# Optimization experiments

Measured on AMD Instinct MI355X. Metric: run time of the kernel, lower is better.

The kernel has to match this reference:

```python
import jax, jax.numpy as jnp
import numpy as np

ND, NPR, DD, DP, LAT, AT, B = 2048, 2048, 128, 128, 128, 32, 16384


def setup_inputs():
    key = jax.random.key(0)
    ks = jax.random.split(key, 20)
    s = 0.05
    d = {}
    d["e_p_adj"] = (jax.random.uniform(ks[0], (ND, NPR)) < 0.05).astype(jnp.float32)
    d["e_e_adj"] = (jax.random.uniform(ks[1], (ND, ND)) < 0.05).astype(jnp.float32)
    d["p_p_adj"] = (jax.random.uniform(ks[2], (NPR, NPR)) < 0.05).astype(jnp.float32)
    d["input_disease"] = jax.random.randint(ks[3], (B,), 0, ND)
    d["input_drug"] = jax.random.randint(ks[4], (B,), 0, NPR)
    d["labels"] = jax.random.randint(ks[5], (B,), 0, 2)
    # learned parameters
    d["disease_emb"] = jax.random.normal(ks[6], (ND, DD)) * s
    d["drug_emb"] = jax.random.normal(ks[7], (NPR, DP)) * s
    d["Wdg"] = jax.random.normal(ks[8], (DP, LAT)) * s   # disease_gcn_w
    d["bdg_lin"] = jnp.zeros((LAT,))                      # Linear bias
    d["bdg"] = jnp.zeros((LAT,))                          # extra disease_gcn_b
    d["Wpg"] = jax.random.normal(ks[9], (DD, LAT)) * s   # drug_gcn_w
    d["bpg_lin"] = jnp.zeros((LAT,))
    d["bpg"] = jnp.zeros((LAT,))
    d["Wa1_d"] = jax.random.normal(ks[10], (DP + DD, AT)) * s  # concat [key(drug), query(disease)]
    d["ba1_d"] = jnp.zeros((AT,))
    d["Wa2_d"] = jax.random.normal(ks[11], (AT, 1)) * s
    d["ba2_d"] = jnp.zeros((1,))
    d["Wa1_p"] = jax.random.normal(ks[12], (DD + DP, AT)) * s  # concat [key(disease), query(drug)]
    d["ba1_p"] = jnp.zeros((AT,))
    d["Wa2_p"] = jax.random.normal(ks[13], (AT, 1)) * s
    d["ba2_p"] = jnp.zeros((1,))
    d["Wd2"] = jax.random.normal(ks[14], (DD, LAT)) * s  # disease_w2
    d["bd2"] = jnp.zeros((LAT,))
    d["Wp3"] = jax.random.normal(ks[15], (DP, LAT)) * s  # drug_w3
    d["bp3"] = jnp.zeros((LAT,))
    d["mlp_W1"] = jax.random.normal(ks[16], (LAT, DD)) * s
    d["mlp_b1"] = jnp.zeros((DD,))
    d["mlp_W2"] = jax.random.normal(ks[17], (DD, DD)) * s
    d["mlp_b2"] = jnp.zeros((DD,))
    d["Wpred"] = jax.random.normal(ks[18], (DD, 1)) * s
    d["bpred"] = jnp.zeros((1,))
    return d


def _attention_gcn(adj, other, selfe, W1, b1, W2, b2):
    # torch: concat([key=other, query=self]) -> Linear(W1) ; split W1 instead of
    # materializing the [Ns, No, Dk+Dq] concat tensor (same math, less HBM traffic)
    do = other.shape[1]
    ko = other @ W1[:do]              # [No, A]
    qs = selfe @ W1[do:]              # [Ns, A]
    h = jax.nn.relu(qs[:, None, :] + ko[None, :, :] + b1)   # [Ns, No, A]
    alpha = jax.nn.relu(jnp.squeeze(h @ W2, -1) + b2[0])    # [Ns, No]
    alpha = alpha * adj
    return jax.nn.softmax(alpha, axis=1) @ other            # [Ns, Do]


def _forward(e_p_adj, e_e_adj, p_p_adj, input_disease, input_drug, labels,
             disease_emb, drug_emb, Wdg, bdg_lin, bdg, Wpg, bpg_lin, bpg,
             Wa1_d, ba1_d, Wa2_d, ba2_d, Wa1_p, ba1_p, Wa2_p, ba2_p,
             Wd2, bd2, Wp3, bp3, mlp_W1, mlp_b1, mlp_W2, mlp_b2, Wpred, bpred):
    h_e_gcn = _attention_gcn(e_p_adj, drug_emb, disease_emb, Wa1_d, ba1_d, Wa2_d, ba2_d)
    h_e_gcn = h_e_gcn @ Wdg + bdg_lin + bdg
    h_p_gcn = _attention_gcn(e_p_adj.T, disease_emb, drug_emb, Wa1_p, ba1_p, Wa2_p, ba2_p)
    h_p_gcn = h_p_gcn @ Wpg + bpg_lin + bpg
    # disease knn branch
    deg_d = jnp.sum(e_e_adj, axis=1, keepdims=True) + 1e-8
    h_e_e = ((e_e_adj @ disease_emb) / deg_d) @ Wd2 + bd2
    h_e = jax.nn.selu(h_e_gcn + h_e_e)
    # drug knn branch
    deg_p = jnp.sum(p_p_adj, axis=1, keepdims=True) + 1e-8
    h_p_p = ((p_p_adj @ drug_emb) / deg_p) @ Wp3 + bp3
    h_p = jax.nn.selu(h_p_gcn + h_p_p)
    # pair prediction MLP
    x = h_e[input_disease] * h_p[input_drug]                # [B, LAT]
    x = jax.nn.selu(x @ mlp_W1 + mlp_b1)
    x = jax.nn.selu(x @ mlp_W2 + mlp_b2)
    z = jnp.squeeze(x @ Wpred, -1) + bpred[0]               # [B]
    y = labels.astype(jnp.float32)
    # BCEWithLogitsLoss (stable), mean reduction
    loss = jnp.mean(jnp.maximum(z, 0.0) - z * y + jnp.log1p(jnp.exp(-jnp.abs(z))))
    return (loss, jax.nn.sigmoid(z))


def reference(e_p_adj, e_e_adj, p_p_adj, input_disease, input_drug, labels,
              disease_emb, drug_emb, Wdg, bdg_lin, bdg, Wpg, bpg_lin, bpg,
              Wa1_d, ba1_d, Wa2_d, ba2_d, Wa1_p, ba1_p, Wa2_p, ba2_p,
              Wd2, bd2, Wp3, bp3, mlp_W1, mlp_b1, mlp_W2, mlp_b2, Wpred, bpred):
    return _forward(e_p_adj, e_e_adj, p_p_adj, input_disease, input_drug, labels,
                    disease_emb, drug_emb, Wdg, bdg_lin, bdg, Wpg, bpg_lin, bpg,
                    Wa1_d, ba1_d, Wa2_d, ba2_d, Wa1_p, ba1_p, Wa2_p, ba2_p,
                    Wd2, bd2, Wp3, bp3, mlp_W1, mlp_b1, mlp_W2, mlp_b2, Wpred, bpred)
```

## Files before the change

### kernel.cpp

```cpp
#include <hip/hip_runtime.h>

#define ND   2048
#define BB   16384

typedef unsigned short u16;
typedef unsigned int u32;
typedef __attribute__((ext_vector_type(8))) short short8;
typedef __attribute__((ext_vector_type(4))) float f32x4;

__device__ inline float bf2f(u16 u) {
    union { u32 i; float f; } v; v.i = ((u32)u) << 16; return v.f;
}
__device__ inline u16 f2bf(float f) {
    union { float f; u32 i; } v; v.f = f;
    u32 i = v.i + 0x7fffu + ((v.i >> 16) & 1u);
    return (u16)(i >> 16);
}
__device__ inline float seluf(float x) {
    const float sc = 1.0507009873554805f, al = 1.6732632423543772f;
    return x > 0.f ? sc * x : sc * al * expm1f(x);
}

__global__ void detectk(const void* __restrict__ demb, u32* __restrict__ flag,
                        u32* __restrict__ cntT, float* __restrict__ lossacc,
                        u32* __restrict__ losscnt) {
    const u16* p = (const u16*)demb;
    int tid = threadIdx.x;
    #pragma unroll
    for (int i = 0; i < 8; i++) cntT[i * 256 + tid] = 0u;
    if (tid == 0) { lossacc[0] = 0.f; losscnt[0] = 0u; }
    int sane = 0;
    #pragma unroll
    for (int i = 0; i < 2; i++) {
        u16 u = p[4 * tid + 2 * i];
        int e = (u >> 7) & 0xFF;
        if (u == 0 || (e >= 0x66 && e <= 0x8C)) sane++;
    }
    __shared__ int red[256];
    red[tid] = sane; __syncthreads();
    for (int o = 128; o > 0; o >>= 1) {
        if (tid < o) red[tid] += red[tid + o];
        __syncthreads();
    }
    if (tid == 0) flag[0] = (red[0] < 300) ? 1u : 0u;
}

#define NSEG 26
struct CvtArgs { const void* src[NSEG]; int off[NSEG]; int n[NSEG]; };
struct CS {
    const void* adj[3];
    u16* ridx[3]; u32* rcnt[3];
};

__global__ __launch_bounds__(256) void cvtcsr(CvtArgs a, u16* __restrict__ base,
                                              CS c, const u32* __restrict__ flag) {
    int bx = blockIdx.x;
    int t = threadIdx.x;
    bool f32 = flag[0] != 0;
    if (bx < 1536) {
        int m = bx >> 9;
        int r0 = (bx & 511) * 4;
        int lane = t & 63;
        __shared__ u32 lcnt[4];
        if (t < 4) lcnt[t] = 0;
        __syncthreads();
        float v[4][8];
        int c0 = t * 8;
        if (f32) {
            #pragma unroll
            for (int rr = 0; rr < 4; rr++) {
                const float4* p = (const float4*)((const float*)c.adj[m] +
                                                  (size_t)(r0 + rr) * 2048 + c0);
                float4 x = p[0], y = p[1];
                v[rr][0] = x.x; v[rr][1] = x.y; v[rr][2] = x.z; v[rr][3] = x.w;
                v[rr][4] = y.x; v[rr][5] = y.y; v[rr][6] = y.z; v[rr][7] = y.w;
            }
        } else {
            #pragma unroll
            for (int rr = 0; rr < 4; rr++) {
                const uint4* p = (const uint4*)((const u16*)c.adj[m] +
                                                (size_t)(r0 + rr) * 2048 + c0);
                uint4 x = p[0];
                u32 u[4] = {x.x, x.y, x.z, x.w};
                #pragma unroll
                for (int i = 0; i < 4; i++) {
                    v[rr][2 * i + 0] = (u[i] & 0xffffu) ? 1.f : 0.f;
                    v[rr][2 * i + 1] = (u[i] >> 16)     ? 1.f : 0.f;
                }
            }
        }
        #pragma unroll
        for (int rr = 0; rr < 4; rr++) {
            int cnt = 0;
            #pragma unroll
            for (int i = 0; i < 8; i++) cnt += (v[rr][i] != 0.f) ? 1 : 0;
            int pfx = cnt;
            #pragma unroll
            for (int o = 1; o < 64; o <<= 1) {
                int s = __shfl_up(pfx, o, 64);
                if (lane >= o) pfx += s;
            }
            int wtot = __shfl(pfx, 63, 64);
            u32 wb = 0;
            if (lane == 0) wb = atomicAdd(&lcnt[rr], (u32)wtot);
            wb = __shfl((int)wb, 0, 64);
            int o = (int)wb + pfx - cnt;
            u16* ridx = c.ridx[m] + (size_t)(r0 + rr) * 2048;
            #pragma unroll
            for (int i = 0; i < 8; i++) {
                if (v[rr][i] != 0.f) ridx[o++] = (u16)(c0 + i);
            }
        }
        __syncthreads();
        if (t < 4) c.rcnt[m][r0 + t] = lcnt[t];
    } else {
        int idx = bx - 1536;
        int seg = idx >> 6, xb = idx & 63;
        int n = a.n[seg];
        const void* s = a.src[seg];
        u16* d = base + a.off[seg];
        int nw = n >> 1;
        if (f32) {
            const float2* sf = (const float2*)s;
            u32* dw = (u32*)d;
            for (int i = xb * 256 + t; i < nw; i += 16384) {
                float2 v = sf[i];
                dw[i] = (u32)f2bf(v.x) | ((u32)f2bf(v.y) << 16);
            }
        } else {
            const u32* sw = (const u32*)s;
            u32* dw = (u32*)d;
            for (int i = xb * 256 + t; i < nw; i += 16384) dw[i] = sw[i];
        }
        if ((n & 1) && xb == 0 && t == 0)
            d[n - 1] = f32 ? f2bf(((const float*)s)[n - 1]) : ((const u16*)s)[n - 1];
    }
}

struct PR {
    const u16* demb; const u16* pemb;
    const u16* Wa1d; const u16* ba1d;
    const u16* Wa1p; const u16* ba1p;
    float* ko_d; float* qs_d; float* ko_p; float* qs_p;
    const u16* idx0; const u32* cnt0; u16* cidx; u32* ccnt;
    const u16* ts[6]; u16* W1T; u16* W2T; u16* WcTe; u16* WcTp;
    const u16* ba[3]; const u16* bb[3]; u16* b_e; u16* b_p;
    float* csd; float* csp;
    const u16* avgidx[2]; const u32* avgcnt[2]; const u16* avgemb[2]; u16* avgout[2];
};

__global__ __launch_bounds__(256) void prep2(PR p) {
    int bx = blockIdx.x;
    int tid = threadIdx.x;
    __shared__ float sx[2][128];
    __shared__ float sred[2][128];
    __shared__ u16 stile[32][33];
    __shared__ float st0[256], st1[256];
    __shared__ u16 Wl[4096];

    if (bx < 4) {
        int id = bx;
        int m = id >> 1, half = id & 1;
        const u16* e = m ? p.pemb : p.demb;
        int c2 = tid & 31, rg = tid >> 5;
        int dbase = half * 64;
        float s0 = 0.f, s1 = 0.f;
        for (int it = 0; it < 256; it++) {
            int row = it * 8 + rg;
            u32 v = *(const u32*)(e + (size_t)row * 128 + dbase + c2 * 2);
            s0 += bf2f((u16)(v & 0xffffu));
            s1 += bf2f((u16)(v >> 16));
        }
        st0[tid] = s0; st1[tid] = s1;
        __syncthreads();
        if (tid < 32) {
            float a0 = 0.f, a1 = 0.f;
            #pragma unroll
            for (int g = 0; g < 8; g++) { a0 += st0[g * 32 + tid]; a1 += st1[g * 32 + tid]; }
            float* cs = m ? p.csp : p.csd;
            cs[dbase + tid * 2 + 0] = a0;
            cs[dbase + tid * 2 + 1] = a1;
        }
        if (tid < 64) {
            int d = dbase + tid;
            if (m == 0)
                p.b_e[d] = f2bf(bf2f(p.ba[0][d]) + bf2f(p.ba[1][d]) + bf2f(p.ba[2][d]));
            else
                p.b_p[d] = f2bf(bf2f(p.bb[0][d]) + bf2f(p.bb[1][d]) + bf2f(p.bb[2][d]));
        }
    } else if (bx < 2052) {
        int r = bx - 4;
        int n = (int)p.cnt0[r];
        const u16* row = p.idx0 + (size_t)r * 2048;
        for (int i = tid; i < n; i += 256) {
            int cc = (int)row[i];
            u32 q = atomicAdd(&p.ccnt[cc], 1u);
            p.cidx[(size_t)cc * 2048 + q] = (u16)r;
        }
    } else if (bx < 3076) {
        int id = bx - 2052;
        int task = id >> 9, blk = id & 511;
        int wv = tid >> 6, lane = tid & 63;
        int grp = lane >> 4, dim = lane & 15;
        int r = blk * 4 + wv;
        const u16* idx = p.avgidx[task] + (size_t)r * 2048;
        int nnz = (int)p.avgcnt[task][r];
        const u16* emb = p.avgemb[task];
        float acc[8];
        #pragma unroll
        for (int t = 0; t < 8; t++) acc[t] = 0.f;
        for (int base = 0; base < nnz; base += 64) {
            int i = base + lane;
            int j = (i < nnz) ? (int)idx[i] : 0;
            int cend = min(64, nnz - base);
            #pragma unroll 4
            for (int k4 = 0; k4 < cend; k4 += 4) {
                int kk = k4 + grp;
                int jk = __shfl(j, kk, 64);
                float wk = (base + kk < nnz) ? 1.f : 0.f;
                const uint4* pp = (const uint4*)((const char*)emb + jk * 256 + dim * 16);
                uint4 vv = *pp;
                u32 u[4] = {vv.x, vv.y, vv.z, vv.w};
                #pragma unroll
                for (int cc = 0; cc < 4; cc++) {
                    acc[2 * cc + 0] = fmaf(wk, bf2f((u16)(u[cc] & 0xffffu)), acc[2 * cc + 0]);
                    acc[2 * cc + 1] = fmaf(wk, bf2f((u16)(u[cc] >> 16)), acc[2 * cc + 1]);
                }
            }
        }
        #pragma unroll
        for (int t = 0; t < 8; t++) {
            acc[t] += __shfl_xor(acc[t], 32, 64);
            acc[t] += __shfl_xor(acc[t], 16, 64);
        }
        if (grp == 0) {
            float sc = 1.f / ((float)nnz + 1e-8f);
            float v[8];
            #pragma unroll
            for (int t = 0; t < 8; t++) v[t] = acc[t] * sc;
            uint4 pk;
            pk.x = (u32)f2bf(v[0]) | ((u32)f2bf(v[1]) << 16);
            pk.y = (u32)f2bf(v[2]) | ((u32)f2bf(v[3]) << 16);
            pk.z = (u32)f2bf(v[4]) | ((u32)f2bf(v[5]) << 16);
            pk.w = (u32)f2bf(v[6]) | ((u32)f2bf(v[7]) << 16);
            *(uint4*)(p.avgout[task] + (size_t)r * 256 + dim * 8) = pk;
        }
    } else if (bx < 4100) {
        int blk = bx - 3076;
        int m = blk >> 8;
        int r0 = (blk & 255) * 8;
        const u16* src; const u16* W; const u16* bias; float* out;
        switch (m) {
            case 0:  src = p.pemb; W = p.Wa1d;            bias = nullptr; out = p.ko_d; break;
            case 1:  src = p.demb; W = p.Wa1d + 128 * 32; bias = p.ba1d;  out = p.qs_d; break;
            case 2:  src = p.demb; W = p.Wa1p;            bias = nullptr; out = p.ko_p; break;
            default: src = p.pemb; W = p.Wa1p + 128 * 32; bias = p.ba1p;  out = p.qs_p; break;
        }
        {
            const uint4* wsrc = (const uint4*)W;
            uint4* wdst = (uint4*)Wl;
            #pragma unroll
            for (int i = 0; i < 2; i++) wdst[i * 256 + tid] = wsrc[i * 256 + tid];
        }
        __syncthreads();
        int sub = tid >> 7, t = tid & 127;
        int a = t & 31, part = t >> 5;
        #pragma unroll 1
        for (int rp = 0; rp < 4; rp++) {
            int row = r0 + rp * 2 + sub;
            sx[sub][t] = bf2f(src[(size_t)row * 128 + t]);
            __syncthreads();
            float s = 0.f;
            #pragma unroll
            for (int k = 0; k < 32; k++)
                s += sx[sub][part * 32 + k] * bf2f(Wl[(part * 32 + k) * 32 + a]);
            sred[sub][t] = s;
            __syncthreads();
            if (part == 0) {
                float tt = sred[sub][a] + sred[sub][a + 32] + sred[sub][a + 64] + sred[sub][a + 96];
                if (bias) tt += bf2f(bias[a]);
                out[(size_t)row * 32 + a] = tt;
            }
            __syncthreads();
        }
    } else {
        int id = bx - 4100;
        int z = id >> 4, rem = id & 15;
        int c0 = (rem & 3) * 32, r0 = (rem >> 2) * 32;
        const u16* in = p.ts[z];
        u16* out; int ldo, ooff;
        switch (z) {
            case 0:  out = p.W1T;  ldo = 128; ooff = 0;   break;
            case 1:  out = p.W2T;  ldo = 128; ooff = 0;   break;
            case 2:  out = p.WcTe; ldo = 256; ooff = 0;   break;
            case 3:  out = p.WcTe; ldo = 256; ooff = 128; break;
            case 4:  out = p.WcTp; ldo = 256; ooff = 0;   break;
            default: out = p.WcTp; ldo = 256; ooff = 128; break;
        }
        int tx = tid & 31, ty = tid >> 5;
        int x = c0 + tx;
        for (int i = ty; i < 32; i += 8)
            stile[i][tx] = in[(size_t)(r0 + i) * 128 + x];
        __syncthreads();
        int rr = r0 + tx;
        for (int i = ty; i < 32; i += 8)
            out[(size_t)(c0 + i) * ldo + ooff + rr] = stile[tx][i];
    }
}

struct SP {
    const u16* idx[2]; const u32* cnt[2];
    const float* ko[2]; const float* qs[2];
    const u16* w2[2]; const u16* b2[2];
    const u16* emb[2]; const float* csum[2];
    u16* out[2];
};

__global__ __launch_bounds__(256) void spagg(SP a) {
    int task = blockIdx.y;
    int tid = threadIdx.x;
    int wv = tid >> 6, lane = tid & 63;
    int grp = lane >> 4, dim = lane & 15;
    int r = blockIdx.x * 4 + wv;
    const u16* idx = a.idx[task] + (size_t)r * 2048;
    int nnz = (int)a.cnt[task][r];
    const u16* emb = a.emb[task];
    const float* ko = a.ko[task];

    float qsr[32], w2h[32];
    {
        const float4* qp = (const float4*)(a.qs[task] + (size_t)r * 32);
        #pragma unroll
        for (int i = 0; i < 8; i++) {
            float4 v = qp[i];
            qsr[4 * i + 0] = v.x; qsr[4 * i + 1] = v.y;
            qsr[4 * i + 2] = v.z; qsr[4 * i + 3] = v.w;
        }
        #pragma unroll
        for (int i = 0; i < 32; i++) w2h[i] = bf2f(a.w2[task][i]);
    }
    float b2v = bf2f(a.b2[task][0]);

    float acc[8];
    #pragma unroll
    for (int t = 0; t < 8; t++) acc[t] = 0.f;
    float wsuml = 0.f;

    for (int base = 0; base < nnz; base += 64) {
        int i = base + lane;
        float w = 0.f;
        int j = 0;
        if (i < nnz) {
            j = (int)idx[i];
            const float4* kp = (const float4*)(ko + (size_t)j * 32);
            float s = 0.f;
            #pragma unroll
            for (int q = 0; q < 8; q++) {
                float4 kv = kp[q];
                s += fmaxf(qsr[4 * q + 0] + kv.x, 0.f) * w2h[4 * q + 0];
                s += fmaxf(qsr[4 * q + 1] + kv.y, 0.f) * w2h[4 * q + 1];
                s += fmaxf(qsr[4 * q + 2] + kv.z, 0.f) * w2h[4 * q + 2];
                s += fmaxf(qsr[4 * q + 3] + kv.w, 0.f) * w2h[4 * q + 3];
            }
            w = __expf(fmaxf(s + b2v, 0.f)) - 1.f;
            wsuml += w;
        }
        int cend = min(64, nnz - base);
        #pragma unroll 4
        for (int k4 = 0; k4 < cend; k4 += 4) {
            int kk = k4 + grp;
            float wk = __shfl(w, kk, 64);
            int jk = __shfl(j, kk, 64);
            const uint4* pp = (const uint4*)((const char*)emb + jk * 256 + dim * 16);
            uint4 vv = *pp;
            u32 u[4] = {vv.x, vv.y, vv.z, vv.w};
            #pragma unroll
            for (int cc = 0; cc < 4; cc++) {
                acc[2 * cc + 0] = fmaf(wk, bf2f((u16)(u[cc] & 0xffffu)), acc[2 * cc + 0]);
                acc[2 * cc + 1] = fmaf(wk, bf2f((u16)(u[cc] >> 16)), acc[2 * cc + 1]);
            }
        }
    }

    #pragma unroll
    for (int t = 0; t < 8; t++) {
        acc[t] += __shfl_xor(acc[t], 32, 64);
        acc[t] += __shfl_xor(acc[t], 16, 64);
    }
    #pragma unroll
    for (int o = 32; o > 0; o >>= 1) wsuml += __shfl_xor(wsuml, o, 64);

    if (grp == 0) {
        float sc = 1.f / (2048.f + wsuml);
        const float* cs = a.csum[task] + dim * 8;
        float v[8];
        #pragma unroll
        for (int t = 0; t < 8; t++) v[t] = (cs[t] + acc[t]) * sc;
        uint4 pk;
        pk.x = (u32)f2bf(v[0]) | ((u32)f2bf(v[1]) << 16);
        pk.y = (u32)f2bf(v[2]) | ((u32)f2bf(v[3]) << 16);
        pk.z = (u32)f2bf(v[4]) | ((u32)f2bf(v[5]) << 16);
        pk.w = (u32)f2bf(v[6]) | ((u32)f2bf(v[7]) << 16);
        *(uint4*)(a.out[task] + (size_t)r * 256 + dim * 8) = pk;
    }
}

struct GD4 {
    const void* A[4]; const u16* BT[4]; u16* C[4];
    const u16* bias[4]; const float* rs[4];
    int lda[4], ldb[4], ldc[4], coff[4], kiters[4], act[4], araw[4], rsmode[4];
};

#define PADK 136

__global__ __launch_bounds__(256, 2) void gemmL(GD4 g, const u32* __restrict__ flag) {
    __shared__ __align__(16) u16 As[16][PADK];
    __shared__ __align__(16) u16 Bs[128][PADK];
    int z = blockIdx.y;
    const void* A = g.A[z];
    const u16* BT = g.BT[z];
    int lda = g.lda[z], ldb = g.ldb[z];
    int kiters = g.kiters[z];
    int tid = threadIdx.x;
    int lane = tid & 63, wv = tid >> 6;
    int mrow = lane & 15, quad = lane >> 4;
    int m0 = blockIdx.x * 16;
    int c0 = wv * 32;
    int sr = tid >> 4, sk = (tid & 15) * 8;
    f32x4 acc0 = {0.f, 0.f, 0.f, 0.f}, acc1 = {0.f, 0.f, 0.f, 0.f};

    short8 ra, rb[8];
    auto ldstage = [&](int kb) {
        ra = *(const short8*)((const u16*)A + (size_t)(m0 + sr) * lda + kb + sk);
        const u16* bbase = BT + (size_t)sr * ldb + kb + sk;
        #pragma unroll
        for (int i = 0; i < 8; i++)
            rb[i] = *(const short8*)(bbase + (size_t)i * 16 * ldb);
    };
    auto ststage = [&]() {
        *(short8*)(&As[sr][sk]) = ra;
        #pragma unroll
        for (int i = 0; i < 8; i++)
            *(short8*)(&Bs[i * 16 + sr][sk]) = rb[i];
    };
    auto compute = [&]() {
        #pragma unroll
        for (int ks = 0; ks < 4; ks++) {
            short8 af = *(const short8*)(&As[mrow][ks * 32 + quad * 8]);
            short8 b0 = *(const short8*)(&Bs[c0 + mrow][ks * 32 + quad * 8]);
            short8 b1 = *(const short8*)(&Bs[c0 + 16 + mrow][ks * 32 + quad * 8]);
            acc0 = __builtin_amdgcn_mfma_f32_16x16x32_bf16(af, b0, acc0, 0, 0, 0);
            acc1 = __builtin_amdgcn_mfma_f32_16x16x32_bf16(af, b1, acc1, 0, 0, 0);
        }
    };

    ldstage(0);
    #pragma unroll 1
    for (int it = 0; it < kiters - 1; ++it) {
        ststage();
        __syncthreads();
        ldstage((it + 1) * 128);
        compute();
        __syncthreads();
    }
    ststage();
    __syncthreads();
    compute();

    const float* rs = g.rs[z];
    int rsmode = g.rsmode[z];
    const u16* bi = g.bias[z];
    u16* C = g.C[z];
    int ldc = g.ldc[z], coff = g.coff[z], act = g.act[z];
    int n0 = c0 + mrow, n1 = n0 + 16;
    float bv0 = bi ? bf2f(bi[n0]) : 0.f;
    float bv1 = bi ? bf2f(bi[n1]) : 0.f;
    #pragma unroll
    for (int r = 0; r < 4; r++) {
        int row = m0 + quad * 4 + r;
        float v0 = acc0[r], v1 = acc1[r];
        if (rsmode == 1) { float sc = rs[row]; v0 *= sc; v1 *= sc; }
        else if (rsmode == 2) {
            float t = 0.f;
            #pragma unroll
            for (int p = 0; p < 8; p++) t += rs[row + p * 2048];
            float sc = 1.f / t;
            v0 *= sc; v1 *= sc;
        }
        v0 += bv0; v1 += bv1;
        if (act) { v0 = seluf(v0); v1 = seluf(v1); }
        C[(size_t)row * ldc + coff + n0] = f2bf(v0);
        C[(size_t)row * ldc + coff + n1] = f2bf(v1);
    }
}

#define PADX 136
__global__ __launch_bounds__(256, 2) void mlpfused(
    const u16* __restrict__ he, const u16* __restrict__ hp,
    const int* __restrict__ di, const int* __restrict__ dr,
    const u16* __restrict__ W1T, const u16* __restrict__ b1,
    const u16* __restrict__ W2T, const u16* __restrict__ b2,
    const u16* __restrict__ wpred, const u16* __restrict__ bpred,
    const int* __restrict__ labels,
    float* __restrict__ out, float* __restrict__ lossacc,
    u32* __restrict__ losscnt) {
    __shared__ __align__(16) u16 Xs[64][PADX];
    __shared__ __align__(16) u16 Ws[128][PADX];
    __shared__ float wred[4];
    int tid = threadIdx.x;
    int lane = tid & 63, wv = tid >> 6;
    int mrow = lane & 15, quad = lane >> 4;
    int p0 = blockIdx.x * 64;

    {
        int row = tid >> 2, sub = tid & 3;
        int b = p0 + row;
        int ia = di[b], ic = dr[b];
        const uint4* pe = (const uint4*)(he + (size_t)ia * 128 + sub * 32);
        const uint4* pp = (const uint4*)(hp + (size_t)ic * 128 + sub * 32);
        #pragma unroll
        for (int q = 0; q < 4; q++) {
            uint4 ue = pe[q], up = pp[q];
            u32 eu[4] = {ue.x, ue.y, ue.z, ue.w};
            u32 pu[4] = {up.x, up.y, up.z, up.w};
            #pragma unroll
            for (int c = 0; c < 4; c++) {
                float lo = bf2f((u16)(eu[c] & 0xffffu)) * bf2f((u16)(pu[c] & 0xffffu));
                float hi = bf2f((u16)(eu[c] >> 16)) * bf2f((u16)(pu[c] >> 16));
                *(u32*)(&Xs[row][sub * 32 + q * 8 + c * 2]) =
                    (u32)f2bf(lo) | ((u32)f2bf(hi) << 16);
            }
        }
    }
    {
        int n = tid >> 1, half = tid & 1;
        const short8* src = (const short8*)(W1T + (size_t)n * 128 + half * 64);
        short8* dst = (short8*)(&Ws[n][half * 64]);
        #pragma unroll
        for (int i = 0; i < 8; i++) dst[i] = src[i];
    }
    __syncthreads();

    f32x4 acc[8];
    #pragma unroll
    for (int nt = 0; nt < 8; nt++) acc[nt] = {0.f, 0.f, 0.f, 0.f};
    #pragma unroll
    for (int ks = 0; ks < 4; ks++) {
        short8 af = *(const short8*)(&Xs[wv * 16 + mrow][ks * 32 + quad * 8]);
        #pragma unroll
        for (int nt = 0; nt < 8; nt++) {
            short8 bfv = *(const short8*)(&Ws[nt * 16 + mrow][ks * 32 + quad * 8]);
            acc[nt] = __builtin_amdgcn_mfma_f32_16x16x32_bf16(af, bfv, acc[nt], 0, 0, 0);
        }
    }
    __syncthreads();
    #pragma unroll
    for (int nt = 0; nt < 8; nt++) {
        int col = nt * 16 + mrow;
        float bv = bf2f(b1[col]);
        #pragma unroll
        for (int r = 0; r < 4; r++) {
            int row = wv * 16 + quad * 4 + r;
            Xs[row][col] = f2bf(seluf(acc[nt][r] + bv));
        }
    }
    {
        int n = tid >> 1, half = tid & 1;
        const short8* src = (const short8*)(W2T + (size_t)n * 128 + half * 64);
        short8* dst = (short8*)(&Ws[n][half * 64]);
        #pragma unroll
        for (int i = 0; i < 8; i++) dst[i] = src[i];
    }
    __syncthreads();

    #pragma unroll
    for (int nt = 0; nt < 8; nt++) acc[nt] = {0.f, 0.f, 0.f, 0.f};
    #pragma unroll
    for (int ks = 0; ks < 4; ks++) {
        short8 af = *(const short8*)(&Xs[wv * 16 + mrow][ks * 32 + quad * 8]);
        #pragma unroll
        for (int nt = 0; nt < 8; nt++) {
            short8 bfv = *(const short8*)(&Ws[nt * 16 + mrow][ks * 32 + quad * 8]);
            acc[nt] = __builtin_amdgcn_mfma_f32_16x16x32_bf16(af, bfv, acc[nt], 0, 0, 0);
        }
    }

    float zp[4] = {0.f, 0.f, 0.f, 0.f};
    #pragma unroll
    for (int nt = 0; nt < 8; nt++) {
        int col = nt * 16 + mrow;
        float bv = bf2f(b2[col]);
        float wp = bf2f(wpred[col]);
        #pragma unroll
        for (int r = 0; r < 4; r++) {
            float x2 = bf2f(f2bf(seluf(acc[nt][r] + bv)));
            zp[r] = fmaf(x2, wp, zp[r]);
        }
    }
    #pragma unroll
    for (int r = 0; r < 4; r++) {
        #pragma unroll
        for (int o = 1; o < 16; o <<= 1) zp[r] += __shfl_xor(zp[r], o, 64);
    }
    float bpv = bf2f(bpred[0]);
    float lsum = 0.f;
    #pragma unroll
    for (int r = 0; r < 4; r++) {
        int b = p0 + wv * 16 + quad * 4 + r;
        float z = zp[r] + bpv;
        float sig = 1.f / (1.f + __expf(-z));
        if (mrow == 0) out[1 + b] = sig;
        float y = (float)labels[b];
        lsum += fmaxf(z, 0.f) - z * y + log1pf(__expf(-fabsf(z)));
    }
    lsum += __shfl_xor(lsum, 16, 64);
    lsum += __shfl_xor(lsum, 32, 64);
    if (lane == 0) wred[wv] = lsum;
    __syncthreads();
    if (tid == 0) {
        float bs = wred[0] + wred[1] + wred[2] + wred[3];
        atomicAdd(lossacc, bs);
        __threadfence();
        u32 old = atomicAdd(losscnt, 1u);
        if (old == 255u) {
            float tot = atomicAdd(lossacc, 0.f);
            out[0] = tot * (1.f / 16384.f);
        }
    }
}

extern "C" void kernel_launch(void* const* d_in, const int* in_sizes, int n_in,
                              void* d_out, int out_size, void* d_ws, size_t ws_size,
                              hipStream_t stream) {
    const void* e_p_adj = d_in[0];
    const void* e_e_adj = d_in[1];
    const void* p_p_adj = d_in[2];
    const int* in_dis  = (const int*)d_in[3];
    const int* in_drug = (const int*)d_in[4];
    const int* labels  = (const int*)d_in[5];
    float* out = (float*)d_out;

    char* ws = (char*)d_ws;
    size_t off = 0;
    auto take = [&](size_t bytes) { char* p = ws + off; off = (off + bytes + 255) & ~(size_t)255; return p; };
    u16*   A_e   = (u16*)take((size_t)2048 * 256 * 2);
    u16*   A_p   = (u16*)take((size_t)2048 * 256 * 2);
    u16*   WcTe  = (u16*)take((size_t)128 * 256 * 2);
    u16*   WcTp  = (u16*)take((size_t)128 * 256 * 2);
    u16*   W1T   = (u16*)take((size_t)128 * 128 * 2);
    u16*   W2T   = (u16*)take((size_t)128 * 128 * 2);
    u16*   b_e   = (u16*)take(256);
    u16*   b_p   = (u16*)take(256);
    u16*   h_e   = (u16*)take((size_t)2048 * 128 * 2);
    u16*   h_p   = (u16*)take((size_t)2048 * 128 * 2);
    float* ko_d  = (float*)take((size_t)2048 * 32 * 4);
    float* qs_d  = (float*)take((size_t)2048 * 32 * 4);
    float* ko_p  = (float*)take((size_t)2048 * 32 * 4);
    float* qs_p  = (float*)take((size_t)2048 * 32 * 4);
    float* csd   = (float*)take(128 * 4);
    float* csp   = (float*)take(128 * 4);
    float* lossacc = (float*)take(256);
    u32*   losscnt = (u32*)((char*)lossacc + 4);
    u32*   flag  = (u32*)take(256);
    u16*   canon = (u16*)take((size_t)700000 * 2);
    u16*   idx0  = (u16*)take((size_t)2048 * 2048 * 2);
    u16*   idx1  = (u16*)take((size_t)2048 * 2048 * 2);
    u16*   idx2  = (u16*)take((size_t)2048 * 2048 * 2);
    u16*   idx3  = (u16*)take((size_t)2048 * 2048 * 2);
    u32*   cnt0  = (u32*)take(2048 * 4);
    u32*   cnt2  = (u32*)take(2048 * 4);
    u32*   cnt3  = (u32*)take(2048 * 4);
    u32*   cntT  = (u32*)take(2048 * 4);

    const int segidx[NSEG] = {6, 7, 14, 18, 8, 22, 11, 24, 26, 28,
                              15, 16, 17, 19, 20, 21,
                              9, 10, 12, 13, 23, 25, 27, 29, 30, 31};
    const int segn[NSEG]   = {262144, 262144, 8192, 8192, 16384, 16384, 16384, 16384, 16384, 16384,
                              32, 32, 1, 32, 32, 1,
                              128, 128, 128, 128, 128, 128, 128, 128, 128, 1};
    CvtArgs ca;
    u16* cp[NSEG];
    {
        int o = 0;
        for (int i = 0; i < NSEG; i++) {
            ca.src[i] = d_in[segidx[i]];
            ca.off[i] = o;
            ca.n[i] = segn[i];
            cp[i] = canon + o;
            o += (segn[i] + 15) & ~15;
        }
    }
    u16 *cdemb = cp[0], *cpemb = cp[1], *cWa1d = cp[2], *cWa1p = cp[3];
    u16 *cWdg = cp[4], *cWd2 = cp[5], *cWpg = cp[6], *cWp3 = cp[7];
    u16 *cW1 = cp[8], *cW2 = cp[9];
    u16 *cba1d = cp[10], *cWa2d = cp[11], *cba2d = cp[12];
    u16 *cba1p = cp[13], *cWa2p = cp[14], *cba2p = cp[15];
    u16 *cbdg_lin = cp[16], *cbdg = cp[17], *cbpg_lin = cp[18], *cbpg = cp[19];
    u16 *cbd2 = cp[20], *cbp3 = cp[21], *cmb1 = cp[22], *cmb2 = cp[23];
    u16 *cWpred = cp[24], *cbpred = cp[25];

    detectk<<<1, 256, 0, stream>>>(d_in[6], flag, cntT, lossacc, losscnt);

    {
        CS cs;
        cs.adj[0] = e_p_adj; cs.ridx[0] = idx0; cs.rcnt[0] = cnt0;
        cs.adj[1] = e_e_adj; cs.ridx[1] = idx2; cs.rcnt[1] = cnt2;
        cs.adj[2] = p_p_adj; cs.ridx[2] = idx3; cs.rcnt[2] = cnt3;
        cvtcsr<<<1536 + 64 * NSEG, 256, 0, stream>>>(ca, canon, cs, flag);
    }

    PR pr;
    pr.demb = cdemb; pr.pemb = cpemb;
    pr.Wa1d = cWa1d; pr.ba1d = cba1d; pr.Wa1p = cWa1p; pr.ba1p = cba1p;
    pr.ko_d = ko_d; pr.qs_d = qs_d; pr.ko_p = ko_p; pr.qs_p = qs_p;
    pr.idx0 = idx0; pr.cnt0 = cnt0; pr.cidx = idx1; pr.ccnt = cntT;
    pr.ts[0] = cW1; pr.ts[1] = cW2; pr.ts[2] = cWdg;
    pr.ts[3] = cWd2; pr.ts[4] = cWpg; pr.ts[5] = cWp3;
    pr.W1T = W1T; pr.W2T = W2T; pr.WcTe = WcTe; pr.WcTp = WcTp;
    pr.ba[0] = cbdg_lin; pr.ba[1] = cbdg; pr.ba[2] = cbd2;
    pr.bb[0] = cbpg_lin; pr.bb[1] = cbpg; pr.bb[2] = cbp3;
    pr.b_e = b_e; pr.b_p = b_p; pr.csd = csd; pr.csp = csp;
    pr.avgidx[0] = idx2; pr.avgcnt[0] = cnt2; pr.avgemb[0] = cdemb; pr.avgout[0] = A_e + 128;
    pr.avgidx[1] = idx3; pr.avgcnt[1] = cnt3; pr.avgemb[1] = cpemb; pr.avgout[1] = A_p + 128;
    prep2<<<4196, 256, 0, stream>>>(pr);

    {
        SP sp;
        sp.idx[0] = idx0; sp.cnt[0] = cnt0; sp.ko[0] = ko_d; sp.qs[0] = qs_d;
        sp.w2[0] = cWa2d; sp.b2[0] = cba2d; sp.emb[0] = cpemb; sp.csum[0] = csp;
        sp.out[0] = A_e;
        sp.idx[1] = idx1; sp.cnt[1] = cntT; sp.ko[1] = ko_p; sp.qs[1] = qs_p;
        sp.w2[1] = cWa2p; sp.b2[1] = cba2p; sp.emb[1] = cdemb; sp.csum[1] = csd;
        sp.out[1] = A_p;
        spagg<<<dim3(512, 2), 256, 0, stream>>>(sp);
    }

    auto setd = [](GD4& g, int z, const void* A, int lda, const u16* BT, int ldb,
                   u16* C, int ldc, int coff, int ki, const u16* bi,
                   const float* rs, int act, int araw, int rm) {
        g.A[z] = A; g.lda[z] = lda; g.BT[z] = BT; g.ldb[z] = ldb;
        g.C[z] = C; g.ldc[z] = ldc; g.coff[z] = coff; g.kiters[z] = ki;
        g.bias[z] = bi; g.rs[z] = rs; g.act[z] = act; g.araw[z] = araw; g.rsmode[z] = rm;
    };

    {
        GD4 g;
        setd(g, 0, A_e, 256, WcTe, 256, h_e, 128, 0, 2, b_e, nullptr, 1, 0, 0);
        setd(g, 1, A_p, 256, WcTp, 256, h_p, 128, 0, 2, b_p, nullptr, 1, 0, 0);
        setd(g, 2, A_e, 256, WcTe, 256, h_e, 128, 0, 2, b_e, nullptr, 1, 0, 0);
        setd(g, 3, A_e, 256, WcTe, 256, h_e, 128, 0, 2, b_e, nullptr, 1, 0, 0);
        gemmL<<<dim3(128, 2), 256, 0, stream>>>(g, flag);
    }

    mlpfused<<<256, 256, 0, stream>>>(h_e, h_p, in_dis, in_drug,
                                      W1T, cmb1, W2T, cmb2,
                                      cWpred, cbpred, labels, out,
                                      lossacc, losscnt);
}
```

Before: 231.7 us.

## Fuse all stages into one persistent kernel with grid-wide barriers

Replaces the chain of separate kernel launches (detect, CSR convert, prep, sparse aggregation, GEMM, MLP) with a single persistent kernel of 512 blocks. Each block strides over the virtual block indices of each stage, and atomic-counter grid barriers separate the stages. Only a tiny init kernel remains. This removes per-launch overhead and the launch gaps between stages, at the cost of spin-wait barriers, occupancy tied to two blocks per CU, and a large shared buffer that all stages reuse.

```diff
diff --git a/kernel.cpp b/kernel.cpp
--- a/kernel.cpp
+++ b/kernel.cpp
@@ -2,11 +2,14 @@
 
 #define ND   2048
 #define BB   16384
+#define NBLK 512
 
 typedef unsigned short u16;
 typedef unsigned int u32;
 typedef __attribute__((ext_vector_type(8))) short short8;
 typedef __attribute__((ext_vector_type(4))) float f32x4;
+typedef u16 urow136[136];
+typedef u16 urow33[33];
 
 __device__ inline float bf2f(u16 u) {
     union { u32 i; float f; } v; v.i = ((u32)u) << 16; return v.f;
@@ -21,203 +24,376 @@
     return x > 0.f ? sc * x : sc * al * expm1f(x);
 }
 
-__global__ void detectk(const void* __restrict__ demb, u32* __restrict__ flag,
-                        u32* __restrict__ cntT, float* __restrict__ lossacc,
-                        u32* __restrict__ losscnt) {
-    const u16* p = (const u16*)demb;
-    int tid = threadIdx.x;
-    #pragma unroll
-    for (int i = 0; i < 8; i++) cntT[i * 256 + tid] = 0u;
-    if (tid == 0) { lossacc[0] = 0.f; losscnt[0] = 0u; }
-    int sane = 0;
-    #pragma unroll
-    for (int i = 0; i < 2; i++) {
-        u16 u = p[4 * tid + 2 * i];
-        int e = (u >> 7) & 0xFF;
-        if (u == 0 || (e >= 0x66 && e <= 0x8C)) sane++;
-    }
-    __shared__ int red[256];
-    red[tid] = sane; __syncthreads();
-    for (int o = 128; o > 0; o >>= 1) {
-        if (tid < o) red[tid] += red[tid + o];
-        __syncthreads();
-    }
-    if (tid == 0) flag[0] = (red[0] < 300) ? 1u : 0u;
-}
-
 #define NSEG 26
-struct CvtArgs { const void* src[NSEG]; int off[NSEG]; int n[NSEG]; };
-struct CS {
+
+struct MG {
     const void* adj[3];
+    const void* demb_raw;
+    const void* src[NSEG]; int soff[NSEG]; int sn[NSEG];
+    u16* canon;
     u16* ridx[3]; u32* rcnt[3];
-};
-
-__global__ __launch_bounds__(256) void cvtcsr(CvtArgs a, u16* __restrict__ base,
-                                              CS c, const u32* __restrict__ flag) {
-    int bx = blockIdx.x;
-    int t = threadIdx.x;
-    bool f32 = flag[0] != 0;
-    if (bx < 1536) {
-        int m = bx >> 9;
-        int r0 = (bx & 511) * 4;
-        int lane = t & 63;
-        __shared__ u32 lcnt[4];
-        if (t < 4) lcnt[t] = 0;
-        __syncthreads();
-        float v[4][8];
-        int c0 = t * 8;
-        if (f32) {
-            #pragma unroll
-            for (int rr = 0; rr < 4; rr++) {
-                const float4* p = (const float4*)((const float*)c.adj[m] +
-                                                  (size_t)(r0 + rr) * 2048 + c0);
-                float4 x = p[0], y = p[1];
-                v[rr][0] = x.x; v[rr][1] = x.y; v[rr][2] = x.z; v[rr][3] = x.w;
-                v[rr][4] = y.x; v[rr][5] = y.y; v[rr][6] = y.z; v[rr][7] = y.w;
-            }
-        } else {
-            #pragma unroll
-            for (int rr = 0; rr < 4; rr++) {
-                const uint4* p = (const uint4*)((const u16*)c.adj[m] +
-                                                (size_t)(r0 + rr) * 2048 + c0);
-                uint4 x = p[0];
-                u32 u[4] = {x.x, x.y, x.z, x.w};
-                #pragma unroll
-                for (int i = 0; i < 4; i++) {
-                    v[rr][2 * i + 0] = (u[i] & 0xffffu) ? 1.f : 0.f;
-                    v[rr][2 * i + 1] = (u[i] >> 16)     ? 1.f : 0.f;
-                }
-            }
-        }
-        #pragma unroll
-        for (int rr = 0; rr < 4; rr++) {
-            int cnt = 0;
-            #pragma unroll
-            for (int i = 0; i < 8; i++) cnt += (v[rr][i] != 0.f) ? 1 : 0;
-            int pfx = cnt;
-            #pragma unroll
-            for (int o = 1; o < 64; o <<= 1) {
-                int s = __shfl_up(pfx, o, 64);
-                if (lane >= o) pfx += s;
-            }
-            int wtot = __shfl(pfx, 63, 64);
-            u32 wb = 0;
-            if (lane == 0) wb = atomicAdd(&lcnt[rr], (u32)wtot);
-            wb = __shfl((int)wb, 0, 64);
-            int o = (int)wb + pfx - cnt;
-            u16* ridx = c.ridx[m] + (size_t)(r0 + rr) * 2048;
-            #pragma unroll
-            for (int i = 0; i < 8; i++) {
-                if (v[rr][i] != 0.f) ridx[o++] = (u16)(c0 + i);
-            }
-        }
-        __syncthreads();
-        if (t < 4) c.rcnt[m][r0 + t] = lcnt[t];
-    } else {
-        int idx = bx - 1536;
-        int seg = idx >> 6, xb = idx & 63;
-        int n = a.n[seg];
-        const void* s = a.src[seg];
-        u16* d = base + a.off[seg];
-        int nw = n >> 1;
-        if (f32) {
-            const float2* sf = (const float2*)s;
-            u32* dw = (u32*)d;
-            for (int i = xb * 256 + t; i < nw; i += 16384) {
-                float2 v = sf[i];
-                dw[i] = (u32)f2bf(v.x) | ((u32)f2bf(v.y) << 16);
-            }
-        } else {
-            const u32* sw = (const u32*)s;
-            u32* dw = (u32*)d;
-            for (int i = xb * 256 + t; i < nw; i += 16384) dw[i] = sw[i];
-        }
-        if ((n & 1) && xb == 0 && t == 0)
-            d[n - 1] = f32 ? f2bf(((const float*)s)[n - 1]) : ((const u16*)s)[n - 1];
-    }
-}
-
-struct PR {
+    u16* cidx; u32* ccnt;
     const u16* demb; const u16* pemb;
-    const u16* Wa1d; const u16* ba1d;
-    const u16* Wa1p; const u16* ba1p;
+    const u16* Wa1d; const u16* ba1d; const u16* Wa1p; const u16* ba1p;
     float* ko_d; float* qs_d; float* ko_p; float* qs_p;
-    const u16* idx0; const u32* cnt0; u16* cidx; u32* ccnt;
     const u16* ts[6]; u16* W1T; u16* W2T; u16* WcTe; u16* WcTp;
     const u16* ba[3]; const u16* bb[3]; u16* b_e; u16* b_p;
     float* csd; float* csp;
     const u16* avgidx[2]; const u32* avgcnt[2]; const u16* avgemb[2]; u16* avgout[2];
+    const u16* sidx[2]; const u32* scnt[2];
+    const float* sko[2]; const float* sqs[2];
+    const u16* sw2[2]; const u16* sb2[2];
+    const u16* semb[2]; const float* scs[2];
+    u16* sout[2];
+    const u16* gA[2]; const u16* gBT[2]; u16* gC[2]; const u16* gbias[2];
+    const int* di; const int* dr;
+    const u16* mb1_; const u16* mb2_;
+    const u16* wpred; const u16* bpred; const int* labels;
+    float* out; float* lossacc;
+    u32* bar;
 };
 
-__global__ __launch_bounds__(256) void prep2(PR p) {
-    int bx = blockIdx.x;
+__device__ inline void gbar(u32* bar, u32 target) {
+    __syncthreads();
+    if (threadIdx.x == 0) {
+        __threadfence();
+        atomicAdd(bar, 1u);
+        while (atomicAdd(bar, 0u) < target)
+            __builtin_amdgcn_s_sleep(2);
+        __threadfence();
+    }
+    __syncthreads();
+}
+
+__global__ void initk(u32* __restrict__ cntT, float* __restrict__ lossacc,
+                      u32* __restrict__ bar) {
     int tid = threadIdx.x;
-    __shared__ float sx[2][128];
-    __shared__ float sred[2][128];
-    __shared__ u16 stile[32][33];
-    __shared__ float st0[256], st1[256];
-    __shared__ u16 Wl[4096];
-
-    if (bx < 4) {
-        int id = bx;
-        int m = id >> 1, half = id & 1;
-        const u16* e = m ? p.pemb : p.demb;
-        int c2 = tid & 31, rg = tid >> 5;
-        int dbase = half * 64;
-        float s0 = 0.f, s1 = 0.f;
-        for (int it = 0; it < 256; it++) {
-            int row = it * 8 + rg;
-            u32 v = *(const u32*)(e + (size_t)row * 128 + dbase + c2 * 2);
-            s0 += bf2f((u16)(v & 0xffffu));
-            s1 += bf2f((u16)(v >> 16));
-        }
-        st0[tid] = s0; st1[tid] = s1;
-        __syncthreads();
-        if (tid < 32) {
-            float a0 = 0.f, a1 = 0.f;
-            #pragma unroll
-            for (int g = 0; g < 8; g++) { a0 += st0[g * 32 + tid]; a1 += st1[g * 32 + tid]; }
-            float* cs = m ? p.csp : p.csd;
-            cs[dbase + tid * 2 + 0] = a0;
-            cs[dbase + tid * 2 + 1] = a1;
-        }
-        if (tid < 64) {
-            int d = dbase + tid;
-            if (m == 0)
-                p.b_e[d] = f2bf(bf2f(p.ba[0][d]) + bf2f(p.ba[1][d]) + bf2f(p.ba[2][d]));
-            else
-                p.b_p[d] = f2bf(bf2f(p.bb[0][d]) + bf2f(p.bb[1][d]) + bf2f(p.bb[2][d]));
-        }
-    } else if (bx < 2052) {
-        int r = bx - 4;
-        int n = (int)p.cnt0[r];
-        const u16* row = p.idx0 + (size_t)r * 2048;
-        for (int i = tid; i < n; i += 256) {
-            int cc = (int)row[i];
-            u32 q = atomicAdd(&p.ccnt[cc], 1u);
-            p.cidx[(size_t)cc * 2048 + q] = (u16)r;
-        }
-    } else if (bx < 3076) {
-        int id = bx - 2052;
-        int task = id >> 9, blk = id & 511;
-        int wv = tid >> 6, lane = tid & 63;
+    #pragma unroll
+    for (int i = 0; i < 8; i++) cntT[i * 256 + tid] = 0u;
+    if (tid == 0) { lossacc[0] = 0.f; bar[0] = 0u; }
+}
+
+__global__ __launch_bounds__(256, 2) void mega(MG g) {
+    int tid = threadIdx.x;
+    int bid = blockIdx.x;
+    int lane = tid & 63, wv = tid >> 6;
+
+    __shared__ __align__(16) char Lraw[52352];
+
+    bool f32;
+    {
+        int* redf = (int*)Lraw;
+        const u16* p6 = (const u16*)g.demb_raw;
+        int sane = 0;
+        #pragma unroll
+        for (int i = 0; i < 2; i++) {
+            u16 u = p6[4 * tid + 2 * i];
+            int e = (u >> 7) & 0xFF;
+            if (u == 0 || (e >= 0x66 && e <= 0x8C)) sane++;
+        }
+        redf[tid] = sane;
+        __syncthreads();
+        for (int o = 128; o > 0; o >>= 1) {
+            if (tid < o) redf[tid] += redf[tid + o];
+            __syncthreads();
+        }
+        f32 = redf[0] < 300;
+        __syncthreads();
+    }
+
+    for (int vb = bid; vb < 3200; vb += NBLK) {
+        if (vb < 1536) {
+            int m = vb >> 9;
+            int r0 = (vb & 511) * 4;
+            u32* lcnt = (u32*)Lraw;
+            if (tid < 4) lcnt[tid] = 0;
+            __syncthreads();
+            float v[4][8];
+            int c0 = tid * 8;
+            if (f32) {
+                #pragma unroll
+                for (int rr = 0; rr < 4; rr++) {
+                    const float4* p = (const float4*)((const float*)g.adj[m] +
+                                                      (size_t)(r0 + rr) * 2048 + c0);
+                    float4 x = p[0], y = p[1];
+                    v[rr][0] = x.x; v[rr][1] = x.y; v[rr][2] = x.z; v[rr][3] = x.w;
+                    v[rr][4] = y.x; v[rr][5] = y.y; v[rr][6] = y.z; v[rr][7] = y.w;
+                }
+            } else {
+                #pragma unroll
+                for (int rr = 0; rr < 4; rr++) {
+                    const uint4* p = (const uint4*)((const u16*)g.adj[m] +
+                                                    (size_t)(r0 + rr) * 2048 + c0);
+                    uint4 x = p[0];
+                    u32 u[4] = {x.x, x.y, x.z, x.w};
+                    #pragma unroll
+                    for (int i = 0; i < 4; i++) {
+                        v[rr][2 * i + 0] = (u[i] & 0xffffu) ? 1.f : 0.f;
+                        v[rr][2 * i + 1] = (u[i] >> 16)     ? 1.f : 0.f;
+                    }
+                }
+            }
+            #pragma unroll
+            for (int rr = 0; rr < 4; rr++) {
+                int cnt = 0;
+                #pragma unroll
+                for (int i = 0; i < 8; i++) cnt += (v[rr][i] != 0.f) ? 1 : 0;
+                int pfx = cnt;
+                #pragma unroll
+                for (int o = 1; o < 64; o <<= 1) {
+                    int s = __shfl_up(pfx, o, 64);
+                    if (lane >= o) pfx += s;
+                }
+                int wtot = __shfl(pfx, 63, 64);
+                u32 wb = 0;
+                if (lane == 0) wb = atomicAdd(&lcnt[rr], (u32)wtot);
+                wb = __shfl((int)wb, 0, 64);
+                int o = (int)wb + pfx - cnt;
+                u16* ridxp = g.ridx[m] + (size_t)(r0 + rr) * 2048;
+                #pragma unroll
+                for (int i = 0; i < 8; i++) {
+                    if (v[rr][i] != 0.f) ridxp[o++] = (u16)(c0 + i);
+                }
+            }
+            __syncthreads();
+            if (tid < 4) g.rcnt[m][r0 + tid] = lcnt[tid];
+        } else {
+            int idx = vb - 1536;
+            int seg = idx >> 6, xb = idx & 63;
+            int n = g.sn[seg];
+            const void* s = g.src[seg];
+            u16* d = g.canon + g.soff[seg];
+            int nw = n >> 1;
+            if (f32) {
+                const float2* sf = (const float2*)s;
+                u32* dw = (u32*)d;
+                for (int i = xb * 256 + tid; i < nw; i += 16384) {
+                    float2 vv = sf[i];
+                    dw[i] = (u32)f2bf(vv.x) | ((u32)f2bf(vv.y) << 16);
+                }
+            } else {
+                const u32* sw = (const u32*)s;
+                u32* dw = (u32*)d;
+                for (int i = xb * 256 + tid; i < nw; i += 16384) dw[i] = sw[i];
+            }
+            if ((n & 1) && xb == 0 && tid == 0)
+                d[n - 1] = f32 ? f2bf(((const float*)s)[n - 1]) : ((const u16*)s)[n - 1];
+        }
+        __syncthreads();
+    }
+    gbar(g.bar, NBLK * 1);
+
+    for (int vb = bid; vb < 4196; vb += NBLK) {
+        if (vb < 4) {
+            float* st0 = (float*)Lraw;
+            float* st1 = (float*)(Lraw + 1024);
+            int m = vb >> 1, half = vb & 1;
+            const u16* e = m ? g.pemb : g.demb;
+            int c2 = tid & 31, rg = tid >> 5;
+            int dbase = half * 64;
+            float s0 = 0.f, s1 = 0.f;
+            for (int it = 0; it < 256; it++) {
+                int row = it * 8 + rg;
+                u32 v = *(const u32*)(e + (size_t)row * 128 + dbase + c2 * 2);
+                s0 += bf2f((u16)(v & 0xffffu));
+                s1 += bf2f((u16)(v >> 16));
+            }
+            st0[tid] = s0; st1[tid] = s1;
+            __syncthreads();
+            if (tid < 32) {
+                float a0 = 0.f, a1 = 0.f;
+                #pragma unroll
+                for (int gg = 0; gg < 8; gg++) { a0 += st0[gg * 32 + tid]; a1 += st1[gg * 32 + tid]; }
+                float* cs = m ? g.csp : g.csd;
+                cs[dbase + tid * 2 + 0] = a0;
+                cs[dbase + tid * 2 + 1] = a1;
+            }
+            if (tid < 64) {
+                int d = dbase + tid;
+                if (m == 0)
+                    g.b_e[d] = f2bf(bf2f(g.ba[0][d]) + bf2f(g.ba[1][d]) + bf2f(g.ba[2][d]));
+                else
+                    g.b_p[d] = f2bf(bf2f(g.bb[0][d]) + bf2f(g.bb[1][d]) + bf2f(g.bb[2][d]));
+            }
+        } else if (vb < 2052) {
+            int r = vb - 4;
+            int n = (int)g.rcnt[0][r];
+            const u16* row = g.ridx[0] + (size_t)r * 2048;
+            for (int i = tid; i < n; i += 256) {
+                int cc = (int)row[i];
+                u32 q = atomicAdd(&g.ccnt[cc], 1u);
+                g.cidx[(size_t)cc * 2048 + q] = (u16)r;
+            }
+        } else if (vb < 3076) {
+            int id = vb - 2052;
+            int task = id >> 9, blk = id & 511;
+            int grp = lane >> 4, dim = lane & 15;
+            int r = blk * 4 + wv;
+            const u16* idx = g.avgidx[task] + (size_t)r * 2048;
+            int nnz = (int)g.avgcnt[task][r];
+            const u16* emb = g.avgemb[task];
+            float acc[8];
+            #pragma unroll
+            for (int t = 0; t < 8; t++) acc[t] = 0.f;
+            for (int base = 0; base < nnz; base += 64) {
+                int i = base + lane;
+                int j = (i < nnz) ? (int)idx[i] : 0;
+                int cend = min(64, nnz - base);
+                #pragma unroll 4
+                for (int k4 = 0; k4 < cend; k4 += 4) {
+                    int kk = k4 + grp;
+                    int jk = __shfl(j, kk, 64);
+                    float wk = (base + kk < nnz) ? 1.f : 0.f;
+                    const uint4* pp = (const uint4*)((const char*)emb + jk * 256 + dim * 16);
+                    uint4 vv = *pp;
+                    u32 u[4] = {vv.x, vv.y, vv.z, vv.w};
+                    #pragma unroll
+                    for (int cc = 0; cc < 4; cc++) {
+                        acc[2 * cc + 0] = fmaf(wk, bf2f((u16)(u[cc] & 0xffffu)), acc[2 * cc + 0]);
+                        acc[2 * cc + 1] = fmaf(wk, bf2f((u16)(u[cc] >> 16)), acc[2 * cc + 1]);
+                    }
+                }
+            }
+            #pragma unroll
+            for (int t = 0; t < 8; t++) {
+                acc[t] += __shfl_xor(acc[t], 32, 64);
+                acc[t] += __shfl_xor(acc[t], 16, 64);
+            }
+            if (grp == 0) {
+                float sc = 1.f / ((float)nnz + 1e-8f);
+                float v[8];
+                #pragma unroll
+                for (int t = 0; t < 8; t++) v[t] = acc[t] * sc;
+                uint4 pk;
+                pk.x = (u32)f2bf(v[0]) | ((u32)f2bf(v[1]) << 16);
+                pk.y = (u32)f2bf(v[2]) | ((u32)f2bf(v[3]) << 16);
+                pk.z = (u32)f2bf(v[4]) | ((u32)f2bf(v[5]) << 16);
+                pk.w = (u32)f2bf(v[6]) | ((u32)f2bf(v[7]) << 16);
+                *(uint4*)(g.avgout[task] + (size_t)r * 256 + dim * 8) = pk;
+            }
+        } else if (vb < 4100) {
+            float* sx = (float*)Lraw;
+            float* sred = (float*)(Lraw + 1024);
+            u16* Wl = (u16*)(Lraw + 2048);
+            int blk = vb - 3076;
+            int m = blk >> 8;
+            int r0 = (blk & 255) * 8;
+            const u16* src; const u16* W; const u16* bias; float* out;
+            switch (m) {
+                case 0:  src = g.pemb; W = g.Wa1d;            bias = nullptr; out = g.ko_d; break;
+                case 1:  src = g.demb; W = g.Wa1d + 128 * 32; bias = g.ba1d;  out = g.qs_d; break;
+                case 2:  src = g.demb; W = g.Wa1p;            bias = nullptr; out = g.ko_p; break;
+                default: src = g.pemb; W = g.Wa1p + 128 * 32; bias = g.ba1p;  out = g.qs_p; break;
+            }
+            {
+                const uint4* wsrc = (const uint4*)W;
+                uint4* wdst = (uint4*)Wl;
+                #pragma unroll
+                for (int i = 0; i < 2; i++) wdst[i * 256 + tid] = wsrc[i * 256 + tid];
+            }
+            __syncthreads();
+            int sub = tid >> 7, t = tid & 127;
+            int a = t & 31, part = t >> 5;
+            #pragma unroll 1
+            for (int rp = 0; rp < 4; rp++) {
+                int row = r0 + rp * 2 + sub;
+                sx[sub * 128 + t] = bf2f(src[(size_t)row * 128 + t]);
+                __syncthreads();
+                float s = 0.f;
+                #pragma unroll
+                for (int k = 0; k < 32; k++)
+                    s += sx[sub * 128 + part * 32 + k] * bf2f(Wl[(part * 32 + k) * 32 + a]);
+                sred[sub * 128 + t] = s;
+                __syncthreads();
+                if (part == 0) {
+                    float tt = sred[sub * 128 + a] + sred[sub * 128 + a + 32] +
+                               sred[sub * 128 + a + 64] + sred[sub * 128 + a + 96];
+                    if (bias) tt += bf2f(bias[a]);
+                    out[(size_t)row * 32 + a] = tt;
+                }
+                __syncthreads();
+            }
+        } else {
+            urow33* stile = (urow33*)Lraw;
+            int id = vb - 4100;
+            int z = id >> 4, rem = id & 15;
+            int c0 = (rem & 3) * 32, r0 = (rem >> 2) * 32;
+            const u16* in = g.ts[z];
+            u16* out; int ldo, ooff;
+            switch (z) {
+                case 0:  out = g.W1T;  ldo = 128; ooff = 0;   break;
+                case 1:  out = g.W2T;  ldo = 128; ooff = 0;   break;
+                case 2:  out = g.WcTe; ldo = 256; ooff = 0;   break;
+                case 3:  out = g.WcTe; ldo = 256; ooff = 128; break;
+                case 4:  out = g.WcTp; ldo = 256; ooff = 0;   break;
+                default: out = g.WcTp; ldo = 256; ooff = 128; break;
+            }
+            int tx = tid & 31, ty = tid >> 5;
+            int x = c0 + tx;
+            for (int i = ty; i < 32; i += 8)
+                stile[i][tx] = in[(size_t)(r0 + i) * 128 + x];
+            __syncthreads();
+            int rr = r0 + tx;
+            for (int i = ty; i < 32; i += 8)
+                out[(size_t)(c0 + i) * ldo + ooff + rr] = stile[tx][i];
+        }
+        __syncthreads();
+    }
+    gbar(g.bar, NBLK * 2);
+
+    for (int vb = bid; vb < 1024; vb += NBLK) {
+        int task = vb >> 9, blk = vb & 511;
         int grp = lane >> 4, dim = lane & 15;
         int r = blk * 4 + wv;
-        const u16* idx = p.avgidx[task] + (size_t)r * 2048;
-        int nnz = (int)p.avgcnt[task][r];
-        const u16* emb = p.avgemb[task];
+        const u16* idx = g.sidx[task] + (size_t)r * 2048;
+        int nnz = (int)g.scnt[task][r];
+        const u16* emb = g.semb[task];
+        const float* ko = g.sko[task];
+
+        float qsr[32], w2h[32];
+        {
+            const float4* qp = (const float4*)(g.sqs[task] + (size_t)r * 32);
+            #pragma unroll
+            for (int i = 0; i < 8; i++) {
+                float4 v = qp[i];
+                qsr[4 * i + 0] = v.x; qsr[4 * i + 1] = v.y;
+                qsr[4 * i + 2] = v.z; qsr[4 * i + 3] = v.w;
+            }
+            #pragma unroll
+            for (int i = 0; i < 32; i++) w2h[i] = bf2f(g.sw2[task][i]);
+        }
+        float b2v = bf2f(g.sb2[task][0]);
+
         float acc[8];
         #pragma unroll
         for (int t = 0; t < 8; t++) acc[t] = 0.f;
+        float wsuml = 0.f;
+
         for (int base = 0; base < nnz; base += 64) {
             int i = base + lane;
-            int j = (i < nnz) ? (int)idx[i] : 0;
+            float w = 0.f;
+            int j = 0;
+            if (i < nnz) {
+                j = (int)idx[i];
+                const float4* kp = (const float4*)(ko + (size_t)j * 32);
+                float s = 0.f;
+                #pragma unroll
+                for (int q = 0; q < 8; q++) {
+                    float4 kv = kp[q];
+                    s += fmaxf(qsr[4 * q + 0] + kv.x, 0.f) * w2h[4 * q + 0];
+                    s += fmaxf(qsr[4 * q + 1] + kv.y, 0.f) * w2h[4 * q + 1];
+                    s += fmaxf(qsr[4 * q + 2] + kv.z, 0.f) * w2h[4 * q + 2];
+                    s += fmaxf(qsr[4 * q + 3] + kv.w, 0.f) * w2h[4 * q + 3];
+                }
+                w = __expf(fmaxf(s + b2v, 0.f)) - 1.f;
+                wsuml += w;
+            }
             int cend = min(64, nnz - base);
             #pragma unroll 4
             for (int k4 = 0; k4 < cend; k4 += 4) {
                 int kk = k4 + grp;
+                float wk = __shfl(w, kk, 64);
                 int jk = __shfl(j, kk, 64);
-                float wk = (base + kk < nnz) ? 1.f : 0.f;
                 const uint4* pp = (const uint4*)((const char*)emb + jk * 256 + dim * 16);
                 uint4 vv = *pp;
                 u32 u[4] = {vv.x, vv.y, vv.z, vv.w};
@@ -233,399 +409,209 @@
             acc[t] += __shfl_xor(acc[t], 32, 64);
             acc[t] += __shfl_xor(acc[t], 16, 64);
         }
+        #pragma unroll
+        for (int o = 32; o > 0; o >>= 1) wsuml += __shfl_xor(wsuml, o, 64);
+
         if (grp == 0) {
-            float sc = 1.f / ((float)nnz + 1e-8f);
+            float sc = 1.f / (2048.f + wsuml);
+            const float* cs = g.scs[task] + dim * 8;
             float v[8];
             #pragma unroll
-            for (int t = 0; t < 8; t++) v[t] = acc[t] * sc;
+            for (int t = 0; t < 8; t++) v[t] = (cs[t] + acc[t]) * sc;
             uint4 pk;
             pk.x = (u32)f2bf(v[0]) | ((u32)f2bf(v[1]) << 16);
             pk.y = (u32)f2bf(v[2]) | ((u32)f2bf(v[3]) << 16);
             pk.z = (u32)f2bf(v[4]) | ((u32)f2bf(v[5]) << 16);
             pk.w = (u32)f2bf(v[6]) | ((u32)f2bf(v[7]) << 16);
-            *(uint4*)(p.avgout[task] + (size_t)r * 256 + dim * 8) = pk;
-        }
-    } else if (bx < 4100) {
-        int blk = bx - 3076;
-        int m = blk >> 8;
-        int r0 = (blk & 255) * 8;
-        const u16* src; const u16* W; const u16* bias; float* out;
-        switch (m) {
-            case 0:  src = p.pemb; W = p.Wa1d;            bias = nullptr; out = p.ko_d; break;
-            case 1:  src = p.demb; W = p.Wa1d + 128 * 32; bias = p.ba1d;  out = p.qs_d; break;
-            case 2:  src = p.demb; W = p.Wa1p;            bias = nullptr; out = p.ko_p; break;
-            default: src = p.pemb; W = p.Wa1p + 128 * 32; bias = p.ba1p;  out = p.qs_p; break;
-        }
+            *(uint4*)(g.sout[task] + (size_t)r * 256 + dim * 8) = pk;
+        }
+    }
+    gbar(g.bar, NBLK * 3);
+
+    for (int vb = bid; vb < 256; vb += NBLK) {
+        urow136* As = (urow136*)Lraw;
+        urow136* Bs = (urow136*)(Lraw + 4352);
+        int z = vb >> 7, bx = vb & 127;
+        const u16* A = g.gA[z];
+        const u16* BT = g.gBT[z];
+        int mrow = lane & 15, quad = lane >> 4;
+        int m0 = bx * 16;
+        int c0 = wv * 32;
+        int sr = tid >> 4, sk = (tid & 15) * 8;
+        f32x4 acc0 = {0.f, 0.f, 0.f, 0.f}, acc1 = {0.f, 0.f, 0.f, 0.f};
+
+        short8 ra, rb[8];
+        auto ldstage = [&](int kb) {
+            ra = *(const short8*)(A + (size_t)(m0 + sr) * 256 + kb + sk);
+            const u16* bbase = BT + (size_t)sr * 256 + kb + sk;
+            #pragma unroll
+            for (int i = 0; i < 8; i++)
+                rb[i] = *(const short8*)(bbase + (size_t)i * 16 * 256);
+        };
+        auto ststage = [&]() {
+            *(short8*)(&As[sr][sk]) = ra;
+            #pragma unroll
+            for (int i = 0; i < 8; i++)
+                *(short8*)(&Bs[i * 16 + sr][sk]) = rb[i];
+        };
+        auto compute = [&]() {
+            #pragma unroll
+            for (int ks = 0; ks < 4; ks++) {
+                short8 af = *(const short8*)(&As[mrow][ks * 32 + quad * 8]);
+                short8 b0 = *(const short8*)(&Bs[c0 + mrow][ks * 32 + quad * 8]);
+                short8 b1 = *(const short8*)(&Bs[c0 + 16 + mrow][ks * 32 + quad * 8]);
+                acc0 = __builtin_amdgcn_mfma_f32_16x16x32_bf16(af, b0, acc0, 0, 0, 0);
+                acc1 = __builtin_amdgcn_mfma_f32_16x16x32_bf16(af, b1, acc1, 0, 0, 0);
+            }
+        };
+
+        ldstage(0);
+        ststage();
+        __syncthreads();
+        ldstage(128);
+        compute();
+        __syncthreads();
+        ststage();
+        __syncthreads();
+        compute();
+
+        const u16* bi = g.gbias[z];
+        u16* C = g.gC[z];
+        int n0 = c0 + mrow, n1 = n0 + 16;
+        float bv0 = bf2f(bi[n0]);
+        float bv1 = bf2f(bi[n1]);
+        #pragma unroll
+        for (int r = 0; r < 4; r++) {
+            int row = m0 + quad * 4 + r;
+            C[(size_t)row * 128 + n0] = f2bf(seluf(acc0[r] + bv0));
+            C[(size_t)row * 128 + n1] = f2bf(seluf(acc1[r] + bv1));
+        }
+        __syncthreads();
+    }
+    gbar(g.bar, NBLK * 4);
+
+    for (int vb = bid; vb < 256; vb += NBLK) {
+        urow136* Xs = (urow136*)Lraw;
+        urow136* Ws = (urow136*)(Lraw + 17408);
+        float* wred = (float*)(Lraw + 52224);
+        int mrow = lane & 15, quad = lane >> 4;
+        int p0 = vb * 64;
+        const u16* he = g.gC[0];
+        const u16* hp = g.gC[1];
+
         {
-            const uint4* wsrc = (const uint4*)W;
-            uint4* wdst = (uint4*)Wl;
-            #pragma unroll
-            for (int i = 0; i < 2; i++) wdst[i * 256 + tid] = wsrc[i * 256 + tid];
-        }
-        __syncthreads();
-        int sub = tid >> 7, t = tid & 127;
-        int a = t & 31, part = t >> 5;
-        #pragma unroll 1
-        for (int rp = 0; rp < 4; rp++) {
-            int row = r0 + rp * 2 + sub;
-            sx[sub][t] = bf2f(src[(size_t)row * 128 + t]);
-            __syncthreads();
-            float s = 0.f;
-            #pragma unroll
-            for (int k = 0; k < 32; k++)
-                s += sx[sub][part * 32 + k] * bf2f(Wl[(part * 32 + k) * 32 + a]);
-            sred[sub][t] = s;
-            __syncthreads();
-            if (part == 0) {
-                float tt = sred[sub][a] + sred[sub][a + 32] + sred[sub][a + 64] + sred[sub][a + 96];
-                if (bias) tt += bf2f(bias[a]);
-                out[(size_t)row * 32 + a] = tt;
-            }
-            __syncthreads();
-        }
-    } else {
-        int id = bx - 4100;
-        int z = id >> 4, rem = id & 15;
-        int c0 = (rem & 3) * 32, r0 = (rem >> 2) * 32;
-        const u16* in = p.ts[z];
-        u16* out; int ldo, ooff;
-        switch (z) {
-            case 0:  out = p.W1T;  ldo = 128; ooff = 0;   break;
-            case 1:  out = p.W2T;  ldo = 128; ooff = 0;   break;
-            case 2:  out = p.WcTe; ldo = 256; ooff = 0;   break;
-            case 3:  out = p.WcTe; ldo = 256; ooff = 128; break;
-            case 4:  out = p.WcTp; ldo = 256; ooff = 0;   break;
-            default: out = p.WcTp; ldo = 256; ooff = 128; break;
-        }
-        int tx = tid & 31, ty = tid >> 5;
-        int x = c0 + tx;
-        for (int i = ty; i < 32; i += 8)
-            stile[i][tx] = in[(size_t)(r0 + i) * 128 + x];
-        __syncthreads();
-        int rr = r0 + tx;
-        for (int i = ty; i < 32; i += 8)
-            out[(size_t)(c0 + i) * ldo + ooff + rr] = stile[tx][i];
-    }
-}
-
-struct SP {
-    const u16* idx[2]; const u32* cnt[2];
-    const float* ko[2]; const float* qs[2];
-    const u16* w2[2]; const u16* b2[2];
-    const u16* emb[2]; const float* csum[2];
-    u16* out[2];
-};
-
-__global__ __launch_bounds__(256) void spagg(SP a) {
-    int task = blockIdx.y;
-    int tid = threadIdx.x;
-    int wv = tid >> 6, lane = tid & 63;
-    int grp = lane >> 4, dim = lane & 15;
-    int r = blockIdx.x * 4 + wv;
-    const u16* idx = a.idx[task] + (size_t)r * 2048;
-    int nnz = (int)a.cnt[task][r];
-    const u16* emb = a.emb[task];
-    const float* ko = a.ko[task];
-
-    float qsr[32], w2h[32];
-    {
-        const float4* qp = (const float4*)(a.qs[task] + (size_t)r * 32);
-        #pragma unroll
-        for (int i = 0; i < 8; i++) {
-            float4 v = qp[i];
-            qsr[4 * i + 0] = v.x; qsr[4 * i + 1] = v.y;
-            qsr[4 * i + 2] = v.z; qsr[4 * i + 3] = v.w;
-        }
-        #pragma unroll
-        for (int i = 0; i < 32; i++) w2h[i] = bf2f(a.w2[task][i]);
-    }
-    float b2v = bf2f(a.b2[task][0]);
-
-    float acc[8];
-    #pragma unroll
-    for (int t = 0; t < 8; t++) acc[t] = 0.f;
-    float wsuml = 0.f;
-
-    for (int base = 0; base < nnz; base += 64) {
-        int i = base + lane;
-        float w = 0.f;
-        int j = 0;
-        if (i < nnz) {
-            j = (int)idx[i];
-            const float4* kp = (const float4*)(ko + (size_t)j * 32);
-            float s = 0.f;
-            #pragma unroll
-            for (int q = 0; q < 8; q++) {
-                float4 kv = kp[q];
-                s += fmaxf(qsr[4 * q + 0] + kv.x, 0.f) * w2h[4 * q + 0];
-                s += fmaxf(qsr[4 * q + 1] + kv.y, 0.f) * w2h[4 * q + 1];
-                s += fmaxf(qsr[4 * q + 2] + kv.z, 0.f) * w2h[4 * q + 2];
-                s += fmaxf(qsr[4 * q + 3] + kv.w, 0.f) * w2h[4 * q + 3];
-            }
-            w = __expf(fmaxf(s + b2v, 0.f)) - 1.f;
-            wsuml += w;
-        }
-        int cend = min(64, nnz - base);
-        #pragma unroll 4
-        for (int k4 = 0; k4 < cend; k4 += 4) {
-            int kk = k4 + grp;
-            float wk = __shfl(w, kk, 64);
-            int jk = __shfl(j, kk, 64);
-            const uint4* pp = (const uint4*)((const char*)emb + jk * 256 + dim * 16);
-            uint4 vv = *pp;
-            u32 u[4] = {vv.x, vv.y, vv.z, vv.w};
-            #pragma unroll
-            for (int cc = 0; cc < 4; cc++) {
-                acc[2 * cc + 0] = fmaf(wk, bf2f((u16)(u[cc] & 0xffffu)), acc[2 * cc + 0]);
-                acc[2 * cc + 1] = fmaf(wk, bf2f((u16)(u[cc] >> 16)), acc[2 * cc + 1]);
-            }
-        }
-    }
-
-    #pragma unroll
-    for (int t = 0; t < 8; t++) {
-        acc[t] += __shfl_xor(acc[t], 32, 64);
-        acc[t] += __shfl_xor(acc[t], 16, 64);
-    }
-    #pragma unroll
-    for (int o = 32; o > 0; o >>= 1) wsuml += __shfl_xor(wsuml, o, 64);
-
-    if (grp == 0) {
-        float sc = 1.f / (2048.f + wsuml);
-        const float* cs = a.csum[task] + dim * 8;
-        float v[8];
-        #pragma unroll
-        for (int t = 0; t < 8; t++) v[t] = (cs[t] + acc[t]) * sc;
-        uint4 pk;
-        pk.x = (u32)f2bf(v[0]) | ((u32)f2bf(v[1]) << 16);
-        pk.y = (u32)f2bf(v[2]) | ((u32)f2bf(v[3]) << 16);
-        pk.z = (u32)f2bf(v[4]) | ((u32)f2bf(v[5]) << 16);
-        pk.w = (u32)f2bf(v[6]) | ((u32)f2bf(v[7]) << 16);
-        *(uint4*)(a.out[task] + (size_t)r * 256 + dim * 8) = pk;
-    }
-}
-
-struct GD4 {
-    const void* A[4]; const u16* BT[4]; u16* C[4];
-    const u16* bias[4]; const float* rs[4];
-    int lda[4], ldb[4], ldc[4], coff[4], kiters[4], act[4], araw[4], rsmode[4];
-};
-
-#define PADK 136
-
-__global__ __launch_bounds__(256, 2) void gemmL(GD4 g, const u32* __restrict__ flag) {
-    __shared__ __align__(16) u16 As[16][PADK];
-    __shared__ __align__(16) u16 Bs[128][PADK];
-    int z = blockIdx.y;
-    const void* A = g.A[z];
-    const u16* BT = g.BT[z];
-    int lda = g.lda[z], ldb = g.ldb[z];
-    int kiters = g.kiters[z];
-    int tid = threadIdx.x;
-    int lane = tid & 63, wv = tid >> 6;
-    int mrow = lane & 15, quad = lane >> 4;
-    int m0 = blockIdx.x * 16;
-    int c0 = wv * 32;
-    int sr = tid >> 4, sk = (tid & 15) * 8;
-    f32x4 acc0 = {0.f, 0.f, 0.f, 0.f}, acc1 = {0.f, 0.f, 0.f, 0.f};
-
-    short8 ra, rb[8];
-    auto ldstage = [&](int kb) {
-        ra = *(const short8*)((const u16*)A + (size_t)(m0 + sr) * lda + kb + sk);
-        const u16* bbase = BT + (size_t)sr * ldb + kb + sk;
-        #pragma unroll
-        for (int i = 0; i < 8; i++)
-            rb[i] = *(const short8*)(bbase + (size_t)i * 16 * ldb);
-    };
-    auto ststage = [&]() {
-        *(short8*)(&As[sr][sk]) = ra;
-        #pragma unroll
-        for (int i = 0; i < 8; i++)
-            *(short8*)(&Bs[i * 16 + sr][sk]) = rb[i];
-    };
-    auto compute = [&]() {
+            int row = tid >> 2, sub = tid & 3;
+            int b = p0 + row;
+            int ia = g.di[b], ic = g.dr[b];
+            const uint4* pe = (const uint4*)(he + (size_t)ia * 128 + sub * 32);
+            const uint4* pp = (const uint4*)(hp + (size_t)ic * 128 + sub * 32);
+            #pragma unroll
+            for (int q = 0; q < 4; q++) {
+                uint4 ue = pe[q], up = pp[q];
+                u32 eu[4] = {ue.x, ue.y, ue.z, ue.w};
+                u32 pu[4] = {up.x, up.y, up.z, up.w};
+                #pragma unroll
+                for (int c = 0; c < 4; c++) {
+                    float lo = bf2f((u16)(eu[c] & 0xffffu)) * bf2f((u16)(pu[c] & 0xffffu));
+                    float hi = bf2f((u16)(eu[c] >> 16)) * bf2f((u16)(pu[c] >> 16));
+                    *(u32*)(&Xs[row][sub * 32 + q * 8 + c * 2]) =
+                        (u32)f2bf(lo) | ((u32)f2bf(hi) << 16);
+                }
+            }
+        }
+        {
+            int n = tid >> 1, half = tid & 1;
+            const short8* src = (const short8*)(g.W1T + (size_t)n * 128 + half * 64);
+            short8* dst = (short8*)(&Ws[n][half * 64]);
+            #pragma unroll
+            for (int i = 0; i < 8; i++) dst[i] = src[i];
+        }
+        __syncthreads();
+
+        f32x4 acc[8];
+        #pragma unroll
+        for (int nt = 0; nt < 8; nt++) acc[nt] = {0.f, 0.f, 0.f, 0.f};
         #pragma unroll
         for (int ks = 0; ks < 4; ks++) {
-            short8 af = *(const short8*)(&As[mrow][ks * 32 + quad * 8]);
-            short8 b0 = *(const short8*)(&Bs[c0 + mrow][ks * 32 + quad * 8]);
-            short8 b1 = *(const short8*)(&Bs[c0 + 16 + mrow][ks * 32 + quad * 8]);
-            acc0 = __builtin_amdgcn_mfma_f32_16x16x32_bf16(af, b0, acc0, 0, 0, 0);
-            acc1 = __builtin_amdgcn_mfma_f32_16x16x32_bf16(af, b1, acc1, 0, 0, 0);
-        }
-    };
-
-    ldstage(0);
-    #pragma unroll 1
-    for (int it = 0; it < kiters - 1; ++it) {
-        ststage();
-        __syncthreads();
-        ldstage((it + 1) * 128);
-        compute();
-        __syncthreads();
-    }
-    ststage();
-    __syncthreads();
-    compute();
-
-    const float* rs = g.rs[z];
-    int rsmode = g.rsmode[z];
-    const u16* bi = g.bias[z];
-    u16* C = g.C[z];
-    int ldc = g.ldc[z], coff = g.coff[z], act = g.act[z];
-    int n0 = c0 + mrow, n1 = n0 + 16;
-    float bv0 = bi ? bf2f(bi[n0]) : 0.f;
-    float bv1 = bi ? bf2f(bi[n1]) : 0.f;
-    #pragma unroll
-    for (int r = 0; r < 4; r++) {
-        int row = m0 + quad * 4 + r;
-        float v0 = acc0[r], v1 = acc1[r];
-        if (rsmode == 1) { float sc = rs[row]; v0 *= sc; v1 *= sc; }
-        else if (rsmode == 2) {
-            float t = 0.f;
-            #pragma unroll
-            for (int p = 0; p < 8; p++) t += rs[row + p * 2048];
-            float sc = 1.f / t;
-            v0 *= sc; v1 *= sc;
-        }
-        v0 += bv0; v1 += bv1;
-        if (act) { v0 = seluf(v0); v1 = seluf(v1); }
-        C[(size_t)row * ldc + coff + n0] = f2bf(v0);
-        C[(size_t)row * ldc + coff + n1] = f2bf(v1);
-    }
-}
-
-#define PADX 136
-__global__ __launch_bounds__(256, 2) void mlpfused(
-    const u16* __restrict__ he, const u16* __restrict__ hp,
-    const int* __restrict__ di, const int* __restrict__ dr,
-    const u16* __restrict__ W1T, const u16* __restrict__ b1,
-    const u16* __restrict__ W2T, const u16* __restrict__ b2,
-    const u16* __restrict__ wpred, const u16* __restrict__ bpred,
-    const int* __restrict__ labels,
-    float* __restrict__ out, float* __restrict__ lossacc,
-    u32* __restrict__ losscnt) {
-    __shared__ __align__(16) u16 Xs[64][PADX];
-    __shared__ __align__(16) u16 Ws[128][PADX];
-    __shared__ float wred[4];
-    int tid = threadIdx.x;
-    int lane = tid & 63, wv = tid >> 6;
-    int mrow = lane & 15, quad = lane >> 4;
-    int p0 = blockIdx.x * 64;
-
-    {
-        int row = tid >> 2, sub = tid & 3;
-        int b = p0 + row;
-        int ia = di[b], ic = dr[b];
-        const uint4* pe = (const uint4*)(he + (size_t)ia * 128 + sub * 32);
-        const uint4* pp = (const uint4*)(hp + (size_t)ic * 128 + sub * 32);
-        #pragma unroll
-        for (int q = 0; q < 4; q++) {
-            uint4 ue = pe[q], up = pp[q];
-            u32 eu[4] = {ue.x, ue.y, ue.z, ue.w};
-            u32 pu[4] = {up.x, up.y, up.z, up.w};
-            #pragma unroll
-            for (int c = 0; c < 4; c++) {
-                float lo = bf2f((u16)(eu[c] & 0xffffu)) * bf2f((u16)(pu[c] & 0xffffu));
-                float hi = bf2f((u16)(eu[c] >> 16)) * bf2f((u16)(pu[c] >> 16));
-                *(u32*)(&Xs[row][sub * 32 + q * 8 + c * 2]) =
-                    (u32)f2bf(lo) | ((u32)f2bf(hi) << 16);
-            }
-        }
-    }
-    {
-        int n = tid >> 1, half = tid & 1;
-        const short8* src = (const short8*)(W1T + (size_t)n * 128 + half * 64);
-        short8* dst = (short8*)(&Ws[n][half * 64]);
-        #pragma unroll
-        for (int i = 0; i < 8; i++) dst[i] = src[i];
-    }
-    __syncthreads();
-
-    f32x4 acc[8];
-    #pragma unroll
-    for (int nt = 0; nt < 8; nt++) acc[nt] = {0.f, 0.f, 0.f, 0.f};
-    #pragma unroll
-    for (int ks = 0; ks < 4; ks++) {
-        short8 af = *(const short8*)(&Xs[wv * 16 + mrow][ks * 32 + quad * 8]);
+            short8 af = *(const short8*)(&Xs[wv * 16 + mrow][ks * 32 + quad * 8]);
+            #pragma unroll
+            for (int nt = 0; nt < 8; nt++) {
+                short8 bfv = *(const short8*)(&Ws[nt * 16 + mrow][ks * 32 + quad * 8]);
+                acc[nt] = __builtin_amdgcn_mfma_f32_16x16x32_bf16(af, bfv, acc[nt], 0, 0, 0);
+            }
+        }
+        __syncthreads();
         #pragma unroll
         for (int nt = 0; nt < 8; nt++) {
-            short8 bfv = *(const short8*)(&Ws[nt * 16 + mrow][ks * 32 + quad * 8]);
-            acc[nt] = __builtin_amdgcn_mfma_f32_16x16x32_bf16(af, bfv, acc[nt], 0, 0, 0);
-        }
-    }
-    __syncthreads();
-    #pragma unroll
-    for (int nt = 0; nt < 8; nt++) {
-        int col = nt * 16 + mrow;
-        float bv = bf2f(b1[col]);
+            int col = nt * 16 + mrow;
+            float bv = bf2f(g.mb1_[col]);
+            #pragma unroll
+            for (int r = 0; r < 4; r++) {
+                int row = wv * 16 + quad * 4 + r;
+                Xs[row][col] = f2bf(seluf(acc[nt][r] + bv));
+            }
+        }
+        {
+            int n = tid >> 1, half = tid & 1;
+            const short8* src = (const short8*)(g.W2T + (size_t)n * 128 + half * 64);
+            short8* dst = (short8*)(&Ws[n][half * 64]);
+            #pragma unroll
+            for (int i = 0; i < 8; i++) dst[i] = src[i];
+        }
+        __syncthreads();
+
+        #pragma unroll
+        for (int nt = 0; nt < 8; nt++) acc[nt] = {0.f, 0.f, 0.f, 0.f};
+        #pragma unroll
+        for (int ks = 0; ks < 4; ks++) {
+            short8 af = *(const short8*)(&Xs[wv * 16 + mrow][ks * 32 + quad * 8]);
+            #pragma unroll
+            for (int nt = 0; nt < 8; nt++) {
+                short8 bfv = *(const short8*)(&Ws[nt * 16 + mrow][ks * 32 + quad * 8]);
+                acc[nt] = __builtin_amdgcn_mfma_f32_16x16x32_bf16(af, bfv, acc[nt], 0, 0, 0);
+            }
+        }
+
+        float zp[4] = {0.f, 0.f, 0.f, 0.f};
+        #pragma unroll
+        for (int nt = 0; nt < 8; nt++) {
+            int col = nt * 16 + mrow;
+            float bv = bf2f(g.mb2_[col]);
+            float wp = bf2f(g.wpred[col]);
+            #pragma unroll
+            for (int r = 0; r < 4; r++) {
+                float x2 = bf2f(f2bf(seluf(acc[nt][r] + bv)));
+                zp[r] = fmaf(x2, wp, zp[r]);
+            }
+        }
         #pragma unroll
         for (int r = 0; r < 4; r++) {
-            int row = wv * 16 + quad * 4 + r;
-            Xs[row][col] = f2bf(seluf(acc[nt][r] + bv));
-        }
-    }
-    {
-        int n = tid >> 1, half = tid & 1;
-        const short8* src = (const short8*)(W2T + (size_t)n * 128 + half * 64);
-        short8* dst = (short8*)(&Ws[n][half * 64]);
-        #pragma unroll
-        for (int i = 0; i < 8; i++) dst[i] = src[i];
-    }
-    __syncthreads();
-
-    #pragma unroll
-    for (int nt = 0; nt < 8; nt++) acc[nt] = {0.f, 0.f, 0.f, 0.f};
-    #pragma unroll
-    for (int ks = 0; ks < 4; ks++) {
-        short8 af = *(const short8*)(&Xs[wv * 16 + mrow][ks * 32 + quad * 8]);
-        #pragma unroll
-        for (int nt = 0; nt < 8; nt++) {
-            short8 bfv = *(const short8*)(&Ws[nt * 16 + mrow][ks * 32 + quad * 8]);
-            acc[nt] = __builtin_amdgcn_mfma_f32_16x16x32_bf16(af, bfv, acc[nt], 0, 0, 0);
-        }
-    }
-
-    float zp[4] = {0.f, 0.f, 0.f, 0.f};
-    #pragma unroll
-    for (int nt = 0; nt < 8; nt++) {
-        int col = nt * 16 + mrow;
-        float bv = bf2f(b2[col]);
-        float wp = bf2f(wpred[col]);
+            #pragma unroll
+            for (int o = 1; o < 16; o <<= 1) zp[r] += __shfl_xor(zp[r], o, 64);
+        }
+        float bpv = bf2f(g.bpred[0]);
+        float lsum = 0.f;
         #pragma unroll
         for (int r = 0; r < 4; r++) {
-            float x2 = bf2f(f2bf(seluf(acc[nt][r] + bv)));
-            zp[r] = fmaf(x2, wp, zp[r]);
-        }
-    }
-    #pragma unroll
-    for (int r = 0; r < 4; r++) {
-        #pragma unroll
-        for (int o = 1; o < 16; o <<= 1) zp[r] += __shfl_xor(zp[r], o, 64);
-    }
-    float bpv = bf2f(bpred[0]);
-    float lsum = 0.f;
-    #pragma unroll
-    for (int r = 0; r < 4; r++) {
-        int b = p0 + wv * 16 + quad * 4 + r;
-        float z = zp[r] + bpv;
-        float sig = 1.f / (1.f + __expf(-z));
-        if (mrow == 0) out[1 + b] = sig;
-        float y = (float)labels[b];
-        lsum += fmaxf(z, 0.f) - z * y + log1pf(__expf(-fabsf(z)));
-    }
-    lsum += __shfl_xor(lsum, 16, 64);
-    lsum += __shfl_xor(lsum, 32, 64);
-    if (lane == 0) wred[wv] = lsum;
-    __syncthreads();
-    if (tid == 0) {
-        float bs = wred[0] + wred[1] + wred[2] + wred[3];
-        atomicAdd(lossacc, bs);
-        __threadfence();
-        u32 old = atomicAdd(losscnt, 1u);
-        if (old == 255u) {
-            float tot = atomicAdd(lossacc, 0.f);
-            out[0] = tot * (1.f / 16384.f);
-        }
+            int b = p0 + wv * 16 + quad * 4 + r;
+            float z = zp[r] + bpv;
+            float sig = 1.f / (1.f + __expf(-z));
+            if (mrow == 0) g.out[1 + b] = sig;
+            float y = (float)g.labels[b];
+            lsum += fmaxf(z, 0.f) - z * y + log1pf(__expf(-fabsf(z)));
+        }
+        lsum += __shfl_xor(lsum, 16, 64);
+        lsum += __shfl_xor(lsum, 32, 64);
+        if (lane == 0) wred[wv] = lsum;
+        __syncthreads();
+        if (tid == 0) atomicAdd(g.lossacc, wred[0] + wred[1] + wred[2] + wred[3]);
+        __syncthreads();
+    }
+    gbar(g.bar, NBLK * 5);
+
+    if (bid == 0 && tid == 0) {
+        float tot = atomicAdd(g.lossacc, 0.f);
+        g.out[0] = tot * (1.f / 16384.f);
     }
 }
 
@@ -660,8 +646,7 @@
     float* csd   = (float*)take(128 * 4);
     float* csp   = (float*)take(128 * 4);
     float* lossacc = (float*)take(256);
-    u32*   losscnt = (u32*)((char*)lossacc + 4);
-    u32*   flag  = (u32*)take(256);
+    u32*   bar   = (u32*)take(256);
     u16*   canon = (u16*)take((size_t)700000 * 2);
     u16*   idx0  = (u16*)take((size_t)2048 * 2048 * 2);
     u16*   idx1  = (u16*)take((size_t)2048 * 2048 * 2);
@@ -678,14 +663,14 @@
     const int segn[NSEG]   = {262144, 262144, 8192, 8192, 16384, 16384, 16384, 16384, 16384, 16384,
                               32, 32, 1, 32, 32, 1,
                               128, 128, 128, 128, 128, 128, 128, 128, 128, 1};
-    CvtArgs ca;
     u16* cp[NSEG];
+    MG mg;
     {
         int o = 0;
         for (int i = 0; i < NSEG; i++) {
-            ca.src[i] = d_in[segidx[i]];
-            ca.off[i] = o;
-            ca.n[i] = segn[i];
+            mg.src[i] = d_in[segidx[i]];
+            mg.soff[i] = o;
+            mg.sn[i] = segn[i];
             cp[i] = canon + o;
             o += (segn[i] + 15) & ~15;
         }
@@ -699,61 +684,37 @@
     u16 *cbd2 = cp[20], *cbp3 = cp[21], *cmb1 = cp[22], *cmb2 = cp[23];
     u16 *cWpred = cp[24], *cbpred = cp[25];
 
-    detectk<<<1, 256, 0, stream>>>(d_in[6], flag, cntT, lossacc, losscnt);
-
-    {
-        CS cs;
-        cs.adj[0] = e_p_adj; cs.ridx[0] = idx0; cs.rcnt[0] = cnt0;
-        cs.adj[1] = e_e_adj; cs.ridx[1] = idx2; cs.rcnt[1] = cnt2;
-        cs.adj[2] = p_p_adj; cs.ridx[2] = idx3; cs.rcnt[2] = cnt3;
-        cvtcsr<<<1536 + 64 * NSEG, 256, 0, stream>>>(ca, canon, cs, flag);
-    }
-
-    PR pr;
-    pr.demb = cdemb; pr.pemb = cpemb;
-    pr.Wa1d = cWa1d; pr.ba1d = cba1d; pr.Wa1p = cWa1p; pr.ba1p = cba1p;
-    pr.ko_d = ko_d; pr.qs_d = qs_d; pr.ko_p = ko_p; pr.qs_p = qs_p;
-    pr.idx0 = idx0; pr.cnt0 = cnt0; pr.cidx = idx1; pr.ccnt = cntT;
-    pr.ts[0] = cW1; pr.ts[1] = cW2; pr.ts[2] = cWdg;
-    pr.ts[3] = cWd2; pr.ts[4] = cWpg; pr.ts[5] = cWp3;
-    pr.W1T = W1T; pr.W2T = W2T; pr.WcTe = WcTe; pr.WcTp = WcTp;
-    pr.ba[0] = cbdg_lin; pr.ba[1] = cbdg; pr.ba[2] = cbd2;
-    pr.bb[0] = cbpg_lin; pr.bb[1] = cbpg; pr.bb[2] = cbp3;
-    pr.b_e = b_e; pr.b_p = b_p; pr.csd = csd; pr.csp = csp;
-    pr.avgidx[0] = idx2; pr.avgcnt[0] = cnt2; pr.avgemb[0] = cdemb; pr.avgout[0] = A_e + 128;
-    pr.avgidx[1] = idx3; pr.avgcnt[1] = cnt3; pr.avgemb[1] = cpemb; pr.avgout[1] = A_p + 128;
-    prep2<<<4196, 256, 0, stream>>>(pr);
-
-    {
-        SP sp;
-        sp.idx[0] = idx0; sp.cnt[0] = cnt0; sp.ko[0] = ko_d; sp.qs[0] = qs_d;
-        sp.w2[0] = cWa2d; sp.b2[0] = cba2d; sp.emb[0] = cpemb; sp.csum[0] = csp;
-        sp.out[0] = A_e;
-        sp.idx[1] = idx1; sp.cnt[1] = cntT; sp.ko[1] = ko_p; sp.qs[1] = qs_p;
-        sp.w2[1] = cWa2p; sp.b2[1] = cba2p; sp.emb[1] = cdemb; sp.csum[1] = csd;
-        sp.out[1] = A_p;
-        spagg<<<dim3(512, 2), 256, 0, stream>>>(sp);
-    }
-
-    auto setd = [](GD4& g, int z, const void* A, int lda, const u16* BT, int ldb,
-                   u16* C, int ldc, int coff, int ki, const u16* bi,
-                   const float* rs, int act, int araw, int rm) {
-        g.A[z] = A; g.lda[z] = lda; g.BT[z] = BT; g.ldb[z] = ldb;
-        g.C[z] = C; g.ldc[z] = ldc; g.coff[z] = coff; g.kiters[z] = ki;
-        g.bias[z] = bi; g.rs[z] = rs; g.act[z] = act; g.araw[z] = araw; g.rsmode[z] = rm;
-    };
-
-    {
-        GD4 g;
-        setd(g, 0, A_e, 256, WcTe, 256, h_e, 128, 0, 2, b_e, nullptr, 1, 0, 0);
-        setd(g, 1, A_p, 256, WcTp, 256, h_p, 128, 0, 2, b_p, nullptr, 1, 0, 0);
-        setd(g, 2, A_e, 256, WcTe, 256, h_e, 128, 0, 2, b_e, nullptr, 1, 0, 0);
-        setd(g, 3, A_e, 256, WcTe, 256, h_e, 128, 0, 2, b_e, nullptr, 1, 0, 0);
-        gemmL<<<dim3(128, 2), 256, 0, stream>>>(g, flag);
-    }
-
-    mlpfused<<<256, 256, 0, stream>>>(h_e, h_p, in_dis, in_drug,
-                                      W1T, cmb1, W2T, cmb2,
-                                      cWpred, cbpred, labels, out,
-                                      lossacc, losscnt);
+    mg.adj[0] = e_p_adj; mg.adj[1] = e_e_adj; mg.adj[2] = p_p_adj;
+    mg.demb_raw = d_in[6];
+    mg.canon = canon;
+    mg.ridx[0] = idx0; mg.ridx[1] = idx2; mg.ridx[2] = idx3;
+    mg.rcnt[0] = cnt0; mg.rcnt[1] = cnt2; mg.rcnt[2] = cnt3;
+    mg.cidx = idx1; mg.ccnt = cntT;
+    mg.demb = cdemb; mg.pemb = cpemb;
+    mg.Wa1d = cWa1d; mg.ba1d = cba1d; mg.Wa1p = cWa1p; mg.ba1p = cba1p;
+    mg.ko_d = ko_d; mg.qs_d = qs_d; mg.ko_p = ko_p; mg.qs_p = qs_p;
+    mg.ts[0] = cW1; mg.ts[1] = cW2; mg.ts[2] = cWdg;
+    mg.ts[3] = cWd2; mg.ts[4] = cWpg; mg.ts[5] = cWp3;
+    mg.W1T = W1T; mg.W2T = W2T; mg.WcTe = WcTe; mg.WcTp = WcTp;
+    mg.ba[0] = cbdg_lin; mg.ba[1] = cbdg; mg.ba[2] = cbd2;
+    mg.bb[0] = cbpg_lin; mg.bb[1] = cbpg; mg.bb[2] = cbp3;
+    mg.b_e = b_e; mg.b_p = b_p; mg.csd = csd; mg.csp = csp;
+    mg.avgidx[0] = idx2; mg.avgcnt[0] = cnt2; mg.avgemb[0] = cdemb; mg.avgout[0] = A_e + 128;
+    mg.avgidx[1] = idx3; mg.avgcnt[1] = cnt3; mg.avgemb[1] = cpemb; mg.avgout[1] = A_p + 128;
+    mg.sidx[0] = idx0; mg.scnt[0] = cnt0; mg.sko[0] = ko_d; mg.sqs[0] = qs_d;
+    mg.sw2[0] = cWa2d; mg.sb2[0] = cba2d; mg.semb[0] = cpemb; mg.scs[0] = csp;
+    mg.sout[0] = A_e;
+    mg.sidx[1] = idx1; mg.scnt[1] = cntT; mg.sko[1] = ko_p; mg.sqs[1] = qs_p;
+    mg.sw2[1] = cWa2p; mg.sb2[1] = cba2p; mg.semb[1] = cdemb; mg.scs[1] = csd;
+    mg.sout[1] = A_p;
+    mg.gA[0] = A_e; mg.gBT[0] = WcTe; mg.gC[0] = h_e; mg.gbias[0] = b_e;
+    mg.gA[1] = A_p; mg.gBT[1] = WcTp; mg.gC[1] = h_p; mg.gbias[1] = b_p;
+    mg.di = in_dis; mg.dr = in_drug;
+    mg.mb1_ = cmb1; mg.mb2_ = cmb2;
+    mg.wpred = cWpred; mg.bpred = cbpred; mg.labels = labels;
+    mg.out = out; mg.lossacc = lossacc;
+    mg.bar = bar;
+
+    initk<<<1, 256, 0, stream>>>(cntT, lossacc, bar);
+    mega<<<NBLK, 256, 0, stream>>>(mg);
 }
```

Result: slower. 492.6 us (+112.6%).
